# Kernel tuning notes

Hardware: AMD Instinct MI355X
Metric: run time of the kernel (lower is better)

## Reference

```python
import jax, jax.numpy as jnp
import numpy as np

B, P, D, H, BOS, C = 64, 8, 1024, 16, 16, 14
S = BOS + C
L, V, HID = 4, 1024, 2048
DH = D // H
TAU, UW = 1.0, 0.1
SOS_IDX, EOS_IDX = 0, 1


def setup_inputs():
    ks = jax.random.split(jax.random.key(0), 16)
    w = lambda k, s: 0.02 * jax.random.normal(k, s, dtype=jnp.float32)
    return {
        "prototypes": jax.random.normal(ks[0], (B, P, D), jnp.float32),
        "query": jax.random.normal(ks[1], (BOS, D), jnp.float32),
        "ca_wq": w(ks[2], (D, D)), "ca_wk": w(ks[3], (D, D)),
        "ca_wv": w(ks[4], (D, D)), "ca_wo": w(ks[5], (D, D)),
        "ln1_w": jnp.ones((L, D)), "ln1_b": jnp.zeros((L, D)),
        "qkv_w": w(ks[6], (L, D, 3 * D)),
        "attn_out_w": w(ks[7], (L, D, D)),
        "rel_bias": w(ks[8], (L, 2 * S - 1, H)),
        "ln2_w": jnp.ones((L, D)), "ln2_b": jnp.zeros((L, D)),
        "mlp_w1": w(ks[9], (L, D, 2 * HID)),
        "mlp_w2": w(ks[10], (L, HID, D)),
        "lnf_w": jnp.ones((D,)), "lnf_b": jnp.zeros((D,)),
        "vocab_w": w(ks[11], (D, V)), "vocab_b": jnp.zeros((V,)),
        "pos_emb": w(ks[12], (C, D)),
        "tok_emb": w(ks[13], (V, D)),
    }


def _ln(x, w, b):
    m = jnp.mean(x, -1, keepdims=True)
    v = jnp.mean(jnp.square(x - m), -1, keepdims=True)
    return (x - m) * jax.lax.rsqrt(v + 1e-5) * w + b


def _forward(prototypes, query, ca_wq, ca_wk, ca_wv, ca_wo, ln1_w, ln1_b, qkv_w,
             attn_out_w, rel_bias, ln2_w, ln2_b, mlp_w1, mlp_w2, lnf_w, lnf_b,
             vocab_w, vocab_b, pos_emb, tok_emb):
    # cross attention (scaling='d' -> divide by head dim) builds the BOS tokens
    qh = (query @ ca_wq).reshape(BOS, H, DH)                 # shared across batch
    kh = (prototypes @ ca_wk).reshape(B, P, H, DH)
    vh = (prototypes @ ca_wv).reshape(B, P, H, DH)
    att = jax.nn.softmax(jnp.einsum('qhd,bkhd->bhqk', qh, kh) / DH, axis=-1)
    bos = jnp.einsum('bhqk,bkhd->bqhd', att, vh).reshape(B, BOS, D) @ ca_wo

    # learned relative position bias -> (L, H, S, S); causal mask (bidirectional=False)
    ridx = jnp.arange(S)[:, None] - jnp.arange(S)[None, :] + (S - 1)
    bias = jnp.transpose(rel_bias[:, ridx], (0, 3, 1, 2))
    causal = jnp.tril(jnp.ones((S, S), dtype=bool))

    def transformer(x):  # pre-LN encoder, SwiGLU MLP (mlp_ratio=2), eval mode
        for l in range(L):
            h = _ln(x, ln1_w[l], ln1_b[l])
            qkv = (h @ qkv_w[l]).reshape(B, S, 3, H, DH)
            sc = jnp.einsum('bqhd,bkhd->bhqk', qkv[:, :, 0], qkv[:, :, 1]) * (DH ** -0.5) + bias[l]
            a = jax.nn.softmax(jnp.where(causal, sc, -1e30), axis=-1)
            x = x + jnp.einsum('bhqk,bkhd->bqhd', a, qkv[:, :, 2]).reshape(B, S, D) @ attn_out_w[l]
            h = _ln(x, ln2_w[l], ln2_b[l])
            u1, u2 = jnp.split(h @ mlp_w1[l], 2, axis=-1)
            x = x + (jax.nn.silu(u1) * u2) @ mlp_w2[l]
        return _ln(x, lnf_w, lnf_b)

    pos_b = jnp.broadcast_to(pos_emb[None], (B, C, D))
    gkey = jax.random.key(42)

    def step(carry, i):
        spoken, _ = carry
        # slots < i hold embedded spoken tokens, slots >= i hold position embeddings
        mask = (jnp.arange(C) < i)[None, :, None]
        x = jnp.concatenate([bos, jnp.where(mask, spoken, pos_b)], axis=1)
        logits = transformer(x)[:, BOS:, :] @ vocab_w + vocab_b
        g = jax.random.gumbel(jax.random.fold_in(gkey, i), logits.shape, logits.dtype)
        soft = jax.nn.softmax((logits + g) / TAU, axis=-1)
        soft = (1.0 - UW) * soft + UW / V
        hard = jax.nn.one_hot(jnp.argmax(soft, axis=-1), V, dtype=soft.dtype)
        st = hard - jax.lax.stop_gradient(soft) + soft  # straight-through one-hot
        return (st @ tok_emb, st), None

    init = (jnp.zeros((B, C, D), jnp.float32), jnp.zeros((B, C, V), jnp.float32))
    (_, st_last), _ = jax.lax.scan(step, init, jnp.arange(C))
    sos = jnp.zeros((B, 1, V), jnp.float32).at[:, 0, SOS_IDX].set(1.0)
    eos = jnp.zeros((B, 1, V), jnp.float32).at[:, 0, EOS_IDX].set(1.0)
    return jnp.concatenate([sos, st_last, eos], axis=1)


def reference(prototypes, query, ca_wq, ca_wk, ca_wv, ca_wo, ln1_w, ln1_b, qkv_w,
              attn_out_w, rel_bias, ln2_w, ln2_b, mlp_w1, mlp_w2, lnf_w, lnf_b,
              vocab_w, vocab_b, pos_emb, tok_emb):
    return _forward(prototypes, query, ca_wq, ca_wk, ca_wv, ca_wo, ln1_w, ln1_b,
                    qkv_w, attn_out_w, rel_bias, ln2_w, ln2_b, mlp_w1, mlp_w2,
                    lnf_w, lnf_b, vocab_w, vocab_b, pos_emb, tok_emb)
```

## Files before the change

### kernel.cpp

```cpp
#include <hip/hip_runtime.h>
#include <stdint.h>
#include <stddef.h>
#include <math.h>

#define NB   64
#define NP   8
#define ND   1024
#define NH   16
#define NBOS 16
#define NC   14
#define NS   30
#define NL   4
#define NV   1024
#define NHID 2048
#define NDH  64

#define JAX_PARTITIONABLE 1

typedef _Float16 half_t;
typedef _Float16 h4_t __attribute__((ext_vector_type(4)));
typedef _Float16 h8_t __attribute__((ext_vector_type(8)));
typedef float f32x4 __attribute__((ext_vector_type(4)));

__device__ __forceinline__ uint32_t rotl32(uint32_t x, int d) {
  return (x << d) | (x >> (32 - d));
}

__device__ __forceinline__ void threefry2x32(uint32_t k0, uint32_t k1,
                                             uint32_t x0, uint32_t x1,
                                             uint32_t& o0, uint32_t& o1) {
  uint32_t ks2 = k0 ^ k1 ^ 0x1BD11BDAu;
  x0 += k0; x1 += k1;
#define TF_R4(a,b,c,d) \
  x0 += x1; x1 = rotl32(x1,(a)); x1 ^= x0; \
  x0 += x1; x1 = rotl32(x1,(b)); x1 ^= x0; \
  x0 += x1; x1 = rotl32(x1,(c)); x1 ^= x0; \
  x0 += x1; x1 = rotl32(x1,(d)); x1 ^= x0;
  TF_R4(13,15,26,6)  x0 += k1;  x1 += ks2 + 1u;
  TF_R4(17,29,16,24) x0 += ks2; x1 += k0 + 2u;
  TF_R4(13,15,26,6)  x0 += k0;  x1 += k1 + 3u;
  TF_R4(17,29,16,24) x0 += k1;  x1 += ks2 + 4u;
  TF_R4(13,15,26,6)  x0 += ks2; x1 += k0 + 5u;
#undef TF_R4
  o0 = x0; o1 = x1;
}

__global__ __launch_bounds__(256) void k_gemm(
    const float* __restrict__ A, const float* __restrict__ Bm,
    float* __restrict__ Cm, const float* __restrict__ bias,
    int M, int N, int K, int epi) {
  __shared__ __align__(16) float As[16][64];
  __shared__ __align__(16) float Bs[16][64];
  const int tid = threadIdx.x;
  const int tx = tid & 15, ty = tid >> 4;
  const int m0 = blockIdx.y * 64, n0 = blockIdx.x * 64;
  const int lar = tid >> 2, lak = (tid & 3) << 2;
  const int lbk = tid >> 4, lbn = (tid & 15) << 2;
  float acc[4][4] = {};
  for (int kt = 0; kt < K; kt += 16) {
    float4 av = make_float4(0.f, 0.f, 0.f, 0.f);
    if (m0 + lar < M)
      av = *(const float4*)(A + (size_t)(m0 + lar) * K + kt + lak);
    float4 bv4 = make_float4(0.f, 0.f, 0.f, 0.f);
    if (n0 + lbn < N)
      bv4 = *(const float4*)(Bm + (size_t)(kt + lbk) * N + n0 + lbn);
    __syncthreads();
    As[lak + 0][lar] = av.x; As[lak + 1][lar] = av.y;
    As[lak + 2][lar] = av.z; As[lak + 3][lar] = av.w;
    *(float4*)(&Bs[lbk][lbn]) = bv4;
    __syncthreads();
#pragma unroll
    for (int kk = 0; kk < 16; ++kk) {
      float4 a4 = *(const float4*)(&As[kk][ty << 2]);
      float4 b4 = *(const float4*)(&Bs[kk][tx << 2]);
      float ar[4] = {a4.x, a4.y, a4.z, a4.w};
      float br[4] = {b4.x, b4.y, b4.z, b4.w};
#pragma unroll
      for (int i2 = 0; i2 < 4; ++i2)
#pragma unroll
        for (int j2 = 0; j2 < 4; ++j2)
          acc[i2][j2] = fmaf(ar[i2], br[j2], acc[i2][j2]);
    }
  }
#pragma unroll
  for (int i2 = 0; i2 < 4; ++i2) {
    int r = m0 + (ty << 2) + i2;
    if (r >= M) continue;
#pragma unroll
    for (int j2 = 0; j2 < 4; ++j2) {
      int c = n0 + (tx << 2) + j2;
      if (c >= N) continue;
      size_t off = (size_t)r * N + c;
      float val = acc[i2][j2];
      if (epi == 1) val += Cm[off];
      else if (epi == 2) val += bias[c];
      Cm[off] = val;
    }
  }
}

__device__ __forceinline__ void gload16(const void* g, const void* l) {
  __builtin_amdgcn_global_load_lds((const __attribute__((address_space(1))) void*)g,
                                   (__attribute__((address_space(3))) void*)l, 16, 0, 0);
}

__device__ __forceinline__ void xcd_swz(int gx, int gy, int& bx, int& by) {
  const int flat = blockIdx.y * gx + blockIdx.x;
  const int chunk = (gx * gy) >> 3;
  const int myid = (flat & 7) * chunk + (flat >> 3);
  bx = myid / gy;
  by = myid % gy;
}

template<int EPI>
__global__ __launch_bounds__(512) void k_g3(
    const half_t* __restrict__ Ah, const half_t* __restrict__ Al,
    const half_t* __restrict__ Bh, const half_t* __restrict__ Bl,
    float* __restrict__ Cout, half_t* __restrict__ Mh, half_t* __restrict__ Ml,
    int M, int N, int K, int CH) {
  __shared__ __align__(16) half_t sAh[2][4096];
  __shared__ __align__(16) half_t sAl[2][4096];
  __shared__ __align__(16) half_t sBh[2][4096];
  __shared__ __align__(16) half_t sBl[2][4096];
  int bx, by; xcd_swz(gridDim.x, gridDim.y, bx, by);
  const int tid = threadIdx.x;
  const int lane = tid & 63, w = tid >> 6;
  const int wm = w >> 2, wn = w & 3;
  const int m0 = by * 128, n0 = bx * 128;
  const int fr = lane & 15, fq = lane >> 4;
  const int kbeg = blockIdx.z * CH;
  const int kend = (kbeg + CH < K) ? (kbeg + CH) : K;
  f32x4 acc[4][2] = {};
  const int r0 = tid >> 2, ch = (tid & 3) * 8;
  const size_t aB = (size_t)(m0 + r0) * K + ch;
  const size_t bB = (size_t)(n0 + r0) * K + ch;
  const int wb = w * 1024;

  auto STAGE = [&](int buf, int kt) {
    gload16(Ah + aB + kt, (char*)(&sAh[buf][0]) + wb);
    gload16(Al + aB + kt, (char*)(&sAl[buf][0]) + wb);
    gload16(Bh + bB + kt, (char*)(&sBh[buf][0]) + wb);
    gload16(Bl + bB + kt, (char*)(&sBl[buf][0]) + wb);
  };

  STAGE(0, kbeg);
  int cur = 0;
  for (int kt = kbeg; kt < kend; kt += 32) {
    const bool has_next = (kt + 32 < kend);
    if (has_next) {
      STAGE(cur ^ 1, kt + 32);
      asm volatile("s_waitcnt vmcnt(4)" ::: "memory");
    } else {
      asm volatile("s_waitcnt vmcnt(0)" ::: "memory");
    }
    asm volatile("s_barrier" ::: "memory");
    const half_t* bAh = &sAh[cur][0] + (wm * 64 + fr) * 32 + fq * 8;
    const half_t* bAl = &sAl[cur][0] + (wm * 64 + fr) * 32 + fq * 8;
    const half_t* bBh = &sBh[cur][0] + (wn * 32 + fr) * 32 + fq * 8;
    const half_t* bBl = &sBl[cur][0] + (wn * 32 + fr) * 32 + fq * 8;
    h8_t a[4], b[2], t[2];
#pragma unroll
    for (int mi = 0; mi < 4; ++mi) a[mi] = *(const h8_t*)(bAh + mi * 512);
#pragma unroll
    for (int ni = 0; ni < 2; ++ni) b[ni] = *(const h8_t*)(bBh + ni * 512);
#pragma unroll
    for (int mi = 0; mi < 4; ++mi)
#pragma unroll
      for (int ni = 0; ni < 2; ++ni)
        acc[mi][ni] = __builtin_amdgcn_mfma_f32_16x16x32_f16(a[mi], b[ni], acc[mi][ni], 0, 0, 0);
#pragma unroll
    for (int ni = 0; ni < 2; ++ni) t[ni] = *(const h8_t*)(bBl + ni * 512);
#pragma unroll
    for (int mi = 0; mi < 4; ++mi)
#pragma unroll
      for (int ni = 0; ni < 2; ++ni)
        acc[mi][ni] = __builtin_amdgcn_mfma_f32_16x16x32_f16(a[mi], t[ni], acc[mi][ni], 0, 0, 0);
#pragma unroll
    for (int mi = 0; mi < 4; ++mi) a[mi] = *(const h8_t*)(bAl + mi * 512);
    asm volatile("s_barrier" ::: "memory");
#pragma unroll
    for (int mi = 0; mi < 4; ++mi)
#pragma unroll
      for (int ni = 0; ni < 2; ++ni)
        acc[mi][ni] = __builtin_amdgcn_mfma_f32_16x16x32_f16(a[mi], b[ni], acc[mi][ni], 0, 0, 0);
    cur ^= 1;
  }
  const float sc = 1.0f / 1024.0f;
  if (EPI == 0) {
    float* Cz = Cout + (size_t)blockIdx.z * M * N;
#pragma unroll
    for (int mi = 0; mi < 4; ++mi) {
      const int row = m0 + wm * 64 + mi * 16 + fq * 4;
#pragma unroll
      for (int ni = 0; ni < 2; ++ni) {
        const int col = n0 + wn * 32 + ni * 16 + fr;
        float* cp = Cz + (size_t)row * N + col;
#pragma unroll
        for (int j = 0; j < 4; ++j) cp[(size_t)j * N] = acc[mi][ni][j] * sc;
      }
    }
  } else if (EPI == 1) {
    const int hid = ((n0 + wn * 32) >> 1) + fr;
#pragma unroll
    for (int mi = 0; mi < 4; ++mi) {
      const int row = m0 + wm * 64 + mi * 16 + fq * 4;
#pragma unroll
      for (int j = 0; j < 4; ++j) {
        const float u1 = acc[mi][0][j] * sc;
        const float u2 = acc[mi][1][j] * sc;
        const float s = 1.0f / (1.0f + expf(-u1));
        const float y = (u1 * s) * u2 * 16.0f;
        const half_t hv = (half_t)y;
        const size_t off = (size_t)(row + j) * NHID + hid;
        Mh[off] = hv;
        Ml[off] = (half_t)(y - (float)hv);
      }
    }
  } else {
#pragma unroll
    for (int mi = 0; mi < 4; ++mi) {
      const int row = m0 + wm * 64 + mi * 16 + fq * 4;
#pragma unroll
      for (int ni = 0; ni < 2; ++ni) {
        const int col = n0 + wn * 32 + ni * 16 + fr;
#pragma unroll
        for (int j = 0; j < 4; ++j) {
          const float v = acc[mi][ni][j] * sc;
          const half_t hv = (half_t)v;
          const size_t off = (size_t)(row + j) * N + col;
          Mh[off] = hv;
          Ml[off] = (half_t)(v - (float)hv);
        }
      }
    }
  }
}

__global__ __launch_bounds__(256) void k_splitw(
    const float* __restrict__ W, half_t* __restrict__ Th, half_t* __restrict__ Tl,
    int K, int N) {
  __shared__ float t[32][33];
  const int kb = blockIdx.x * 32, nb = blockIdx.y * 32;
  const int tid = threadIdx.x;
  const int rr = tid >> 5, cc = tid & 31;
#pragma unroll
  for (int i = 0; i < 4; ++i)
    t[rr + i * 8][cc] = W[(size_t)(kb + rr + i * 8) * N + nb + cc];
  __syncthreads();
#pragma unroll
  for (int i = 0; i < 4; ++i) {
    const int nr = rr + i * 8;
    const float x = t[cc][nr] * 64.0f;
    const half_t h = (half_t)x;
    const float r = x - (float)h;
    const size_t off = (size_t)(nb + nr) * K + kb + cc;
    Th[off] = h;
    Tl[off] = (half_t)r;
  }
}

__global__ __launch_bounds__(256) void k_splitw_swz(
    const float* __restrict__ W, half_t* __restrict__ Th, half_t* __restrict__ Tl,
    int K, int N) {
  __shared__ float t[32][33];
  const int kb = blockIdx.x * 32, nb = blockIdx.y * 32;
  const int tid = threadIdx.x;
  const int rr = tid >> 5, cc = tid & 31;
#pragma unroll
  for (int i = 0; i < 4; ++i)
    t[rr + i * 8][cc] = W[(size_t)(kb + rr + i * 8) * N + nb + cc];
  __syncthreads();
#pragma unroll
  for (int i = 0; i < 4; ++i) {
    const int n = nb + rr + i * 8;
    const int hid = n & (NHID - 1), half = n >> 11;
    const int p = ((hid >> 4) << 5) + (half << 4) + (hid & 15);
    const float x = t[cc][rr + i * 8] * 64.0f;
    const half_t h = (half_t)x;
    const float r = x - (float)h;
    const size_t off = (size_t)p * K + kb + cc;
    Th[off] = h;
    Tl[off] = (half_t)r;
  }
}

__global__ __launch_bounds__(256) void k_ca_attn(
    const float* __restrict__ qh, const float* __restrict__ kh,
    const float* __restrict__ vh, float* __restrict__ bosw) {
  const int b = blockIdx.x >> 4, h = blockIdx.x & 15;
  __shared__ float q[NBOS][NDH], kk[NP][NDH], vv[NP][NDH], a[NBOS][NP];
  const int tid = threadIdx.x;
  for (int idx = tid; idx < NBOS * NDH; idx += 256) {
    int qi = idx >> 6, d = idx & 63;
    q[qi][d] = qh[(size_t)qi * ND + h * NDH + d];
  }
  for (int idx = tid; idx < NP * NDH; idx += 256) {
    int p = idx >> 6, d = idx & 63;
    kk[p][d] = kh[(size_t)(b * NP + p) * ND + h * NDH + d];
    vv[p][d] = vh[(size_t)(b * NP + p) * ND + h * NDH + d];
  }
  __syncthreads();
  if (tid < NBOS * NP) {
    int qi = tid >> 3, p = tid & 7;
    float dot = 0.f;
    for (int d = 0; d < NDH; ++d) dot = fmaf(q[qi][d], kk[p][d], dot);
    a[qi][p] = dot / 64.0f;
  }
  __syncthreads();
  if (tid < NBOS) {
    float mx = a[tid][0];
    for (int p = 1; p < NP; ++p) mx = fmaxf(mx, a[tid][p]);
    float sum = 0.f;
    for (int p = 0; p < NP; ++p) { float e = expf(a[tid][p] - mx); a[tid][p] = e; sum += e; }
    for (int p = 0; p < NP; ++p) a[tid][p] /= sum;
  }
  __syncthreads();
  for (int idx = tid; idx < NBOS * NDH; idx += 256) {
    int qi = idx >> 6, d = idx & 63;
    float o = 0.f;
    for (int p = 0; p < NP; ++p) o = fmaf(a[qi][p], vv[p][d], o);
    bosw[(size_t)(b * NBOS + qi) * ND + h * NDH + d] = o;
  }
}

__global__ __launch_bounds__(256) void k_attn(
    const float* __restrict__ qkv, const float* __restrict__ relb,
    float* __restrict__ attout) {
  const int b = blockIdx.x >> 4, h = blockIdx.x & 15;
  __shared__ float q[NS][NDH], kk[NS][NDH], vv[NS][NDH];
  __shared__ float a[NS][NS];
  const int tid = threadIdx.x;
  for (int idx = tid; idx < NS * NDH; idx += 256) {
    int s = idx >> 6, d = idx & 63;
    size_t base = ((size_t)(b * NS + s) * 3) * ND + h * NDH + d;
    q[s][d]  = qkv[base];
    kk[s][d] = qkv[base + ND];
    vv[s][d] = qkv[base + 2 * ND];
  }
  __syncthreads();
  for (int idx = tid; idx < NS * NS; idx += 256) {
    int i = idx / NS, j = idx % NS;
    float sc = 0.f;
    if (j <= i) {
      float dot = 0.f;
      for (int d = 0; d < NDH; ++d) dot = fmaf(q[i][d], kk[j][d], dot);
      sc = dot * 0.125f + relb[(size_t)(i - j + NS - 1) * NH + h];
    }
    a[i][j] = sc;
  }
  __syncthreads();
  if (tid < NS) {
    const int i = tid;
    float mx = -INFINITY;
    for (int j = 0; j <= i; ++j) mx = fmaxf(mx, a[i][j]);
    float sum = 0.f;
    for (int j = 0; j <= i; ++j) { float e = expf(a[i][j] - mx); a[i][j] = e; sum += e; }
    for (int j = 0; j <= i; ++j) a[i][j] /= sum;
    for (int j = i + 1; j < NS; ++j) a[i][j] = 0.f;
  }
  __syncthreads();
  for (int idx = tid; idx < NS * NDH; idx += 256) {
    int i = idx >> 6, d = idx & 63;
    float o = 0.f;
    for (int j = 0; j < NS; ++j) o = fmaf(a[i][j], vv[j][d], o);
    attout[(size_t)(b * NS + i) * ND + h * NDH + d] = o;
  }
}

__global__ __launch_bounds__(256) void k_attn16p(
    const half_t* __restrict__ Qh, const half_t* __restrict__ Ql,
    const float* __restrict__ relb,
    half_t* __restrict__ Oh, half_t* __restrict__ Ol, int S) {
  const int b = blockIdx.x >> 4, h = blockIdx.x & 15;
  __shared__ float q[NS][NDH], kk[NS][NDH], vv[NS][NDH];
  __shared__ float a[NS][NS];
  const int tid = threadIdx.x;
  for (int idx = tid; idx < S * NDH; idx += 256) {
    int s = idx >> 6, d = idx & 63;
    size_t base = (size_t)(b * S + s) * 3072 + h * NDH + d;
    q[s][d]  = (float)Qh[base] + (float)Ql[base];
    kk[s][d] = (float)Qh[base + 1024] + (float)Ql[base + 1024];
    vv[s][d] = (float)Qh[base + 2048] + (float)Ql[base + 2048];
  }
  __syncthreads();
  for (int idx = tid; idx < S * S; idx += 256) {
    int i = idx / S, j = idx % S;
    float sc = 0.f;
    if (j <= i) {
      float dot = 0.f;
      for (int d = 0; d < NDH; ++d) dot = fmaf(q[i][d], kk[j][d], dot);
      sc = dot * 0.125f + relb[(size_t)(i - j + NS - 1) * NH + h];
    }
    a[i][j] = sc;
  }
  __syncthreads();
  if (tid < S) {
    const int i = tid;
    float mx = -INFINITY;
    for (int j = 0; j <= i; ++j) mx = fmaxf(mx, a[i][j]);
    float sum = 0.f;
    for (int j = 0; j <= i; ++j) { float e = expf(a[i][j] - mx); a[i][j] = e; sum += e; }
    for (int j = 0; j <= i; ++j) a[i][j] /= sum;
    for (int j = i + 1; j < S; ++j) a[i][j] = 0.f;
  }
  __syncthreads();
  for (int idx = tid; idx < S * NDH; idx += 256) {
    int i = idx >> 6, d = idx & 63;
    float o = 0.f;
    for (int j = 0; j < S; ++j) o = fmaf(a[i][j], vv[j][d], o);
    const float y = o * 16.0f;
    const half_t hv = (half_t)y;
    const size_t off = (size_t)(b * S + i) * ND + h * NDH + d;
    Oh[off] = hv;
    Ol[off] = (half_t)(y - (float)hv);
  }
}

__global__ __launch_bounds__(256) void k_copy_kv(
    const half_t* __restrict__ Qh, const half_t* __restrict__ Ql,
    half_t* __restrict__ Ch, half_t* __restrict__ Cl) {
  const int row = blockIdx.x;
  const int c0 = threadIdx.x * 8;
  const size_t src = (size_t)row * 3072 + 1024 + c0;
  const size_t dst = (size_t)row * 2048 + c0;
  *(h8_t*)(Ch + dst) = *(const h8_t*)(Qh + src);
  *(h8_t*)(Cl + dst) = *(const h8_t*)(Ql + src);
}

__global__ __launch_bounds__(256) void k_attn16c(
    const half_t* __restrict__ Qh, const half_t* __restrict__ Ql,
    const half_t* __restrict__ Ch, const half_t* __restrict__ Cl,
    const float* __restrict__ relb,
    half_t* __restrict__ Oh, half_t* __restrict__ Ol, int ncur) {
  const int b = blockIdx.x >> 4, h = blockIdx.x & 15;
  const int S = NBOS + ncur;
  __shared__ float q[NC][NDH], kk[NS][NDH], vv[NS][NDH];
  __shared__ float a[NC][NS];
  const int tid = threadIdx.x;
  for (int idx = tid; idx < ncur * NDH; idx += 256) {
    int c = idx >> 6, d = idx & 63;
    size_t base = (size_t)(b * ncur + c) * 3072 + h * NDH + d;
    q[c][d] = (float)Qh[base] + (float)Ql[base];
  }
  for (int idx = tid; idx < S * NDH; idx += 256) {
    int j = idx >> 6, d = idx & 63;
    if (j < NBOS) {
      size_t r = (size_t)(b * NBOS + j) * 2048 + h * NDH + d;
      kk[j][d] = (float)Ch[r] + (float)Cl[r];
      vv[j][d] = (float)Ch[r + 1024] + (float)Cl[r + 1024];
    } else {
      size_t base = (size_t)(b * ncur + (j - NBOS)) * 3072 + h * NDH + d;
      kk[j][d] = (float)Qh[base + 1024] + (float)Ql[base + 1024];
      vv[j][d] = (float)Qh[base + 2048] + (float)Ql[base + 2048];
    }
  }
  __syncthreads();
  for (int idx = tid; idx < ncur * S; idx += 256) {
    int c = idx / S, j = idx % S;
    const int s = NBOS + c;
    float sc = 0.f;
    if (j <= s) {
      float dot = 0.f;
      for (int d = 0; d < NDH; ++d) dot = fmaf(q[c][d], kk[j][d], dot);
      sc = dot * 0.125f + relb[(size_t)(s - j + NS - 1) * NH + h];
    }
    a[c][j] = sc;
  }
  __syncthreads();
  if (tid < ncur) {
    const int c = tid, s = NBOS + c;
    float mx = -INFINITY;
    for (int j = 0; j <= s; ++j) mx = fmaxf(mx, a[c][j]);
    float sum = 0.f;
    for (int j = 0; j <= s; ++j) { float e = expf(a[c][j] - mx); a[c][j] = e; sum += e; }
    for (int j = 0; j <= s; ++j) a[c][j] /= sum;
    for (int j = s + 1; j < S; ++j) a[c][j] = 0.f;
  }
  __syncthreads();
  for (int idx = tid; idx < ncur * NDH; idx += 256) {
    int c = idx >> 6, d = idx & 63;
    float o = 0.f;
    for (int j = 0; j < S; ++j) o = fmaf(a[c][j], vv[j][d], o);
    const float y = o * 16.0f;
    const half_t hv = (half_t)y;
    const size_t off = (size_t)(b * ncur + c) * ND + h * NDH + d;
    Oh[off] = hv;
    Ol[off] = (half_t)(y - (float)hv);
  }
}

__device__ __forceinline__ float block_sum(float val, float* sbuf) {
  for (int off = 32; off > 0; off >>= 1) val += __shfl_down(val, off, 64);
  const int wid = threadIdx.x >> 6;
  if ((threadIdx.x & 63) == 0) sbuf[wid] = val;
  __syncthreads();
  if (threadIdx.x == 0) sbuf[0] = sbuf[0] + sbuf[1] + sbuf[2] + sbuf[3];
  __syncthreads();
  float r = sbuf[0];
  __syncthreads();
  return r;
}

__device__ __forceinline__ void ln_core_emit16(
    float4 x4, const float* w, const float* bvec, float* sbuf,
    half_t* Oh, half_t* Ol, size_t rowoff, int d0) {
  float mean = block_sum(x4.x + x4.y + x4.z + x4.w, sbuf) * (1.0f / 1024.0f);
  float dx0 = x4.x - mean, dx1 = x4.y - mean, dx2 = x4.z - mean, dx3 = x4.w - mean;
  float var = block_sum(dx0*dx0 + dx1*dx1 + dx2*dx2 + dx3*dx3, sbuf) * (1.0f / 1024.0f);
  float rs = 1.0f / sqrtf(var + 1e-5f);
  float4 w4 = *(const float4*)(w + d0);
  float4 b4 = *(const float4*)(bvec + d0);
  float y0 = (dx0 * rs * w4.x + b4.x) * 16.0f;
  float y1 = (dx1 * rs * w4.y + b4.y) * 16.0f;
  float y2 = (dx2 * rs * w4.z + b4.z) * 16.0f;
  float y3 = (dx3 * rs * w4.w + b4.w) * 16.0f;
  h4_t vh, vl;
  vh.x = (half_t)y0; vl.x = (half_t)(y0 - (float)vh.x);
  vh.y = (half_t)y1; vl.y = (half_t)(y1 - (float)vh.y);
  vh.z = (half_t)y2; vl.z = (half_t)(y2 - (float)vh.z);
  vh.w = (half_t)y3; vl.w = (half_t)(y3 - (float)vh.w);
  *(h4_t*)(Oh + rowoff + d0) = vh;
  *(h4_t*)(Ol + rowoff + d0) = vl;
}

__global__ __launch_bounds__(256) void k_ln(
    const float* __restrict__ in, const float* __restrict__ w,
    const float* __restrict__ bvec, float* __restrict__ out) {
  __shared__ float sbuf[4];
  const size_t row = blockIdx.x;
  const int d0 = threadIdx.x << 2;
  float4 x4 = *(const float4*)(in + row * ND + d0);
  float mean = block_sum(x4.x + x4.y + x4.z + x4.w, sbuf) * (1.0f / 1024.0f);
  float dx0 = x4.x - mean, dx1 = x4.y - mean, dx2 = x4.z - mean, dx3 = x4.w - mean;
  float var = block_sum(dx0*dx0 + dx1*dx1 + dx2*dx2 + dx3*dx3, sbuf) * (1.0f / 1024.0f);
  float rs = 1.0f / sqrtf(var + 1e-5f);
  float4 w4 = *(const float4*)(w + d0);
  float4 b4 = *(const float4*)(bvec + d0);
  float4 o;
  o.x = dx0 * rs * w4.x + b4.x;
  o.y = dx1 * rs * w4.y + b4.y;
  o.z = dx2 * rs * w4.z + b4.z;
  o.w = dx3 * rs * w4.w + b4.w;
  *(float4*)(out + row * ND + d0) = o;
}

template<int WRITEX>
__global__ __launch_bounds__(256) void k_red_ln(
    const float* __restrict__ parts, float* __restrict__ X,
    const float* __restrict__ w, const float* __restrict__ bvec,
    half_t* __restrict__ Oh, half_t* __restrict__ Ol, int Mp) {
  __shared__ float sbuf[4];
  const size_t row = blockIdx.x;
  const int d0 = threadIdx.x << 2;
  const size_t off = row * ND + d0;
  const size_t MN = (size_t)Mp * 1024;
  float4 x4 = *(const float4*)(X + off);
  float4 p0 = *(const float4*)(parts + off);
  float4 p1 = *(const float4*)(parts + MN + off);
  float4 p2 = *(const float4*)(parts + 2 * MN + off);
  x4.x += p0.x + p1.x + p2.x; x4.y += p0.y + p1.y + p2.y;
  x4.z += p0.z + p1.z + p2.z; x4.w += p0.w + p1.w + p2.w;
  if (WRITEX) *(float4*)(X + off) = x4;
  ln_core_emit16(x4, w, bvec, sbuf, Oh, Ol, row * ND, d0);
}

__global__ __launch_bounds__(256) void k_lnf(
    const float* __restrict__ x, const float* __restrict__ w,
    const float* __restrict__ bvec, float* __restrict__ out) {
  __shared__ float sbuf[4];
  const int blk = blockIdx.x;
  const int b = blk / NC, c = blk % NC;
  const size_t row = (size_t)b * NS + NBOS + c;
  const int d0 = threadIdx.x << 2;
  float4 x4 = *(const float4*)(x + row * ND + d0);
  float mean = block_sum(x4.x + x4.y + x4.z + x4.w, sbuf) * (1.0f / 1024.0f);
  float dx0 = x4.x - mean, dx1 = x4.y - mean, dx2 = x4.z - mean, dx3 = x4.w - mean;
  float var = block_sum(dx0*dx0 + dx1*dx1 + dx2*dx2 + dx3*dx3, sbuf) * (1.0f / 1024.0f);
  float rs = 1.0f / sqrtf(var + 1e-5f);
  float4 w4 = *(const float4*)(w + d0);
  float4 b4 = *(const float4*)(bvec + d0);
  float4 o;
  o.x = dx0 * rs * w4.x + b4.x;
  o.y = dx1 * rs * w4.y + b4.y;
  o.z = dx2 * rs * w4.z + b4.z;
  o.w = dx3 * rs * w4.w + b4.w;
  *(float4*)(out + (size_t)blk * ND + d0) = o;
}

__device__ __forceinline__ float4 build_row(
    const float* bos, const float* pos_emb, const float* tok_emb,
    const int* tok, const float* stval, int b, int s, int d0, int step) {
  float4 o;
  if (s < NBOS) {
    o = *(const float4*)(bos + (size_t)(b * NBOS + s) * ND + d0);
  } else {
    int j = s - NBOS;
    if (j < step) {
      float sv = stval[b * NC + j];
      int t = tok[b * NC + j];
      float4 e = *(const float4*)(tok_emb + (size_t)t * ND + d0);
      o.x = sv * e.x; o.y = sv * e.y; o.z = sv * e.z; o.w = sv * e.w;
    } else {
      o = *(const float4*)(pos_emb + (size_t)j * ND + d0);
    }
  }
  return o;
}

__global__ __launch_bounds__(256) void k_build_x(
    const float* __restrict__ bos, const float* __restrict__ pos_emb,
    const float* __restrict__ tok_emb, const int* __restrict__ tok,
    const float* __restrict__ stval, float* __restrict__ x, int step) {
  const int row = blockIdx.x;
  const int b = row / NS, s = row % NS;
  const int d0 = threadIdx.x << 2;
  float4 o = build_row(bos, pos_emb, tok_emb, tok, stval, b, s, d0, step);
  *(float4*)(x + (size_t)row * ND + d0) = o;
}

__global__ __launch_bounds__(256) void k_build_ln(
    const float* __restrict__ bos, const float* __restrict__ pos_emb,
    const float* __restrict__ tok_emb, const int* __restrict__ tok,
    const float* __restrict__ stval, const float* __restrict__ w,
    const float* __restrict__ bvec, float* __restrict__ x,
    half_t* __restrict__ Oh, half_t* __restrict__ Ol, int step, int S) {
  __shared__ float sbuf[4];
  const int row = blockIdx.x;
  const int b = row / S, s = row % S;
  const int d0 = threadIdx.x << 2;
  float4 o = build_row(bos, pos_emb, tok_emb, tok, stval, b, s, d0, step);
  *(float4*)(x + (size_t)row * ND + d0) = o;
  ln_core_emit16(o, w, bvec, sbuf, Oh, Ol, (size_t)row * ND, d0);
}

__global__ __launch_bounds__(256) void k_build_ln_c(
    const float* __restrict__ pos_emb, const float* __restrict__ tok_emb,
    const int* __restrict__ tok, const float* __restrict__ stval,
    const float* __restrict__ w, const float* __restrict__ bvec,
    float* __restrict__ x, half_t* __restrict__ Oh, half_t* __restrict__ Ol,
    int step, int ncur) {
  __shared__ float sbuf[4];
  const int row = blockIdx.x;
  const int b = row / ncur, c = row % ncur;
  const int d0 = threadIdx.x << 2;
  float4 o;
  if (c < step) {
    float sv = stval[b * NC + c];
    int t = tok[b * NC + c];
    float4 e = *(const float4*)(tok_emb + (size_t)t * ND + d0);
    o.x = sv * e.x; o.y = sv * e.y; o.z = sv * e.z; o.w = sv * e.w;
  } else {
    o = *(const float4*)(pos_emb + (size_t)c * ND + d0);
  }
  *(float4*)(x + (size_t)row * ND + d0) = o;
  ln_core_emit16(o, w, bvec, sbuf, Oh, Ol, (size_t)row * ND, d0);
}

__global__ __launch_bounds__(256) void k_swiglu(const float* __restrict__ u,
                                                float* __restrict__ m) {
  const size_t idx4 = (size_t)blockIdx.x * 256 + threadIdx.x;
  const size_t row = idx4 >> 9;
  const size_t c0 = (idx4 & 511) << 2;
  const float* ur = u + row * (2 * NHID);
  float4 a4 = *(const float4*)(ur + c0);
  float4 b4 = *(const float4*)(ur + NHID + c0);
  float4 o;
  { float s = 1.0f / (1.0f + expf(-a4.x)); o.x = (a4.x * s) * b4.x; }
  { float s = 1.0f / (1.0f + expf(-a4.y)); o.y = (a4.y * s) * b4.y; }
  { float s = 1.0f / (1.0f + expf(-a4.z)); o.z = (a4.z * s) * b4.z; }
  { float s = 1.0f / (1.0f + expf(-a4.w)); o.w = (a4.w * s) * b4.w; }
  *(float4*)(m + row * NHID + c0) = o;
}

template<int GRED>
__global__ __launch_bounds__(256) void k_gumbel_t(
    const float* __restrict__ logits, const float* __restrict__ vb,
    int* __restrict__ tok, float* __restrict__ stval, float* __restrict__ out,
    int step, int finalstep, int ncur, int Mp) {
  const int blk = blockIdx.x;
  const int b = blk / ncur, c = blk % ncur;
  const int tid = threadIdx.x;
  uint32_t fk0, fk1;
  threefry2x32(0u, 42u, 0u, (uint32_t)step, fk0, fk1);
  const float* zrow = logits + (size_t)blk * NV;
  const size_t MN = (size_t)Mp * 1024;
  float y[4];
  float bv = -INFINITY; int bi = 0;
#pragma unroll
  for (int j = 0; j < 4; ++j) {
    const int v = tid + (j << 8);
    const uint32_t idx = (uint32_t)(b * NC + c) * 1024u + (uint32_t)v;
    uint32_t o0, o1, bits;
#if JAX_PARTITIONABLE
    threefry2x32(fk0, fk1, 0u, idx, o0, o1);
    bits = o0 ^ o1;
#else
    const uint32_t half = (uint32_t)(NB * NC * NV / 2);
    uint32_t jj = (idx < half) ? idx : idx - half;
    threefry2x32(fk0, fk1, jj, jj + half, o0, o1);
    bits = (idx < half) ? o0 : o1;
#endif
    float f = __uint_as_float(0x3F800000u | (bits >> 9)) - 1.0f;
    float uu = (f == 0.0f) ? 1.17549435e-38f : f;
    float g = -logf(-logf(uu));
    float z;
    if (GRED) z = zrow[v] + zrow[MN + v] + zrow[2 * MN + v] + vb[v];
    else      z = zrow[v];
    float yv = z + g;
    y[j] = yv;
    if (yv > bv) { bv = yv; bi = v; }
  }
  __shared__ float swv[4]; __shared__ int swi[4];
  __shared__ float s_ymax; __shared__ int s_arg;
  for (int off = 32; off > 0; off >>= 1) {
    float ov = __shfl_down(bv, off, 64);
    int   oi = __shfl_down(bi, off, 64);
    if (ov > bv || (ov == bv && oi < bi)) { bv = ov; bi = oi; }
  }
  if ((tid & 63) == 0) { swv[tid >> 6] = bv; swi[tid >> 6] = bi; }
  __syncthreads();
  if (tid == 0) {
    float mv = swv[0]; int mi = swi[0];
    for (int w2 = 1; w2 < 4; ++w2)
      if (swv[w2] > mv || (swv[w2] == mv && swi[w2] < mi)) { mv = swv[w2]; mi = swi[w2]; }
    s_ymax = mv; s_arg = mi;
  }
  __syncthreads();
  const float ymax = s_ymax;
  float es = 0.f;
#pragma unroll
  for (int j = 0; j < 4; ++j) es += expf(y[j] - ymax);
  __shared__ float sbuf2[4]; __shared__ float s_es;
  for (int off = 32; off > 0; off >>= 1) es += __shfl_down(es, off, 64);
  if ((tid & 63) == 0) sbuf2[tid >> 6] = es;
  __syncthreads();
  if (tid == 0) s_es = sbuf2[0] + sbuf2[1] + sbuf2[2] + sbuf2[3];
  __syncthreads();
  const float esum = s_es;
  const float sprob = 0.9f * (1.0f / esum) + (0.1f / 1024.0f);
  const float stv = (1.0f - sprob) + sprob;
  if (tid == 0) { tok[b * NC + c] = s_arg; stval[b * NC + c] = stv; }
  if (finalstep) {
    float* orow = out + ((size_t)b * (NC + 2) + 1 + c) * NV;
#pragma unroll
    for (int j = 0; j < 4; ++j) {
      const int v = tid + (j << 8);
      orow[v] = (v == s_arg) ? stv : 0.0f;
    }
  }
}

__global__ __launch_bounds__(256) void k_out_init(float* __restrict__ out) {
  const int b = blockIdx.x;
  const int tid = threadIdx.x;
#pragma unroll
  for (int j = 0; j < 4; ++j) {
    const int v = tid + (j << 8);
    out[((size_t)b * (NC + 2) + 0) * NV + v]      = (v == 0) ? 1.0f : 0.0f;
    out[((size_t)b * (NC + 2) + NC + 1) * NV + v] = (v == 1) ? 1.0f : 0.0f;
  }
}

extern "C" void kernel_launch(void* const* d_in, const int* in_sizes, int n_in,
                              void* d_out, int out_size, void* d_ws, size_t ws_size,
                              hipStream_t stream) {
  (void)in_sizes; (void)n_in; (void)out_size;
  const float* prototypes = (const float*)d_in[0];
  const float* query      = (const float*)d_in[1];
  const float* ca_wq      = (const float*)d_in[2];
  const float* ca_wk      = (const float*)d_in[3];
  const float* ca_wv      = (const float*)d_in[4];
  const float* ca_wo      = (const float*)d_in[5];
  const float* ln1_w      = (const float*)d_in[6];
  const float* ln1_b      = (const float*)d_in[7];
  const float* qkv_w      = (const float*)d_in[8];
  const float* attn_out_w = (const float*)d_in[9];
  const float* rel_bias   = (const float*)d_in[10];
  const float* ln2_w      = (const float*)d_in[11];
  const float* ln2_b      = (const float*)d_in[12];
  const float* mlp_w1     = (const float*)d_in[13];
  const float* mlp_w2     = (const float*)d_in[14];
  const float* lnf_w      = (const float*)d_in[15];
  const float* lnf_b      = (const float*)d_in[16];
  const float* vocab_w    = (const float*)d_in[17];
  const float* vocab_b    = (const float*)d_in[18];
  const float* pos_emb    = (const float*)d_in[19];
  const float* tok_emb    = (const float*)d_in[20];
  float* out = (float*)d_out;

  dim3 thr(256);
  dim3 thr512(512);
  const size_t NEED = 234889216ull;

  if (ws_size >= NEED) {
    char* p = (char*)d_ws;
    auto alloc = [&](size_t bytes) { char* r = p; p += (bytes + 255) & ~(size_t)255; return r; };
    half_t *WqH[NL], *WqL[NL], *WaH[NL], *WaL[NL], *W1H[NL], *W1L[NL], *W2H[NL], *W2L[NL];
    for (int l = 0; l < NL; ++l) {
      WqH[l] = (half_t*)alloc(3072 * 1024 * 2);
      WqL[l] = (half_t*)alloc(3072 * 1024 * 2);
      WaH[l] = (half_t*)alloc(1024 * 1024 * 2);
      WaL[l] = (half_t*)alloc(1024 * 1024 * 2);
      W1H[l] = (half_t*)alloc(4096 * 1024 * 2);
      W1L[l] = (half_t*)alloc(4096 * 1024 * 2);
      W2H[l] = (half_t*)alloc(1024 * 2048 * 2);
      W2L[l] = (half_t*)alloc(1024 * 2048 * 2);
    }
    half_t* WvH = (half_t*)alloc(1024 * 1024 * 2);
    half_t* WvL = (half_t*)alloc(1024 * 1024 * 2);
    half_t *KVh[NL], *KVl[NL];
    for (int l = 0; l < NL; ++l) {
      KVh[l] = (half_t*)alloc(1024 * 2048 * 2);
      KVl[l] = (half_t*)alloc(1024 * 2048 * 2);
    }
    half_t* Hh  = (half_t*)alloc(1024 * 1024 * 2);
    half_t* Hl  = (half_t*)alloc(1024 * 1024 * 2);
    float*  X   = (float*)alloc(1024 * 1024 * 4);
    char*  QKVr = alloc(12582912);
    half_t* Mh  = (half_t*)alloc(1024 * 2048 * 2);
    half_t* Ml  = (half_t*)alloc(1024 * 2048 * 2);
    float* STV  = (float*)alloc(4096);
    int*   TOK  = (int*)alloc(4096);
    float* PARTS = (float*)QKVr;
    half_t* QKVh = (half_t*)QKVr;
    half_t* QKVl = QKVh + (size_t)1024 * 3072;
    float* BOSb  = (float*)Mh;

    for (int l = 0; l < NL; ++l) {
      k_splitw<<<dim3(32, 96), thr, 0, stream>>>(qkv_w + (size_t)l * ND * 3 * ND, WqH[l], WqL[l], 1024, 3072);
      k_splitw<<<dim3(32, 32), thr, 0, stream>>>(attn_out_w + (size_t)l * ND * ND, WaH[l], WaL[l], 1024, 1024);
      k_splitw_swz<<<dim3(32, 128), thr, 0, stream>>>(mlp_w1 + (size_t)l * ND * 2 * NHID, W1H[l], W1L[l], 1024, 4096);
      k_splitw<<<dim3(64, 32), thr, 0, stream>>>(mlp_w2 + (size_t)l * NHID * ND, W2H[l], W2L[l], 2048, 1024);
    }
    k_splitw<<<dim3(32, 32), thr, 0, stream>>>(vocab_w, WvH, WvL, 1024, 1024);

    float* QH = (float*)QKVr;
    float* KH = (float*)QKVr + 16384;
    float* VH = (float*)QKVr + 540672;
    float* BOSW = (float*)QKVr + 1064960;
    k_gemm<<<dim3(16, 1),  thr, 0, stream>>>(query,      ca_wq, QH,   nullptr, NBOS,    ND, ND, 0);
    k_gemm<<<dim3(16, 8),  thr, 0, stream>>>(prototypes, ca_wk, KH,   nullptr, NB * NP, ND, ND, 0);
    k_gemm<<<dim3(16, 8),  thr, 0, stream>>>(prototypes, ca_wv, VH,   nullptr, NB * NP, ND, ND, 0);
    k_ca_attn<<<dim3(NB * NH), thr, 0, stream>>>(QH, KH, VH, BOSW);
    k_gemm<<<dim3(16, 16), thr, 0, stream>>>(BOSW, ca_wo, BOSb, nullptr, NB * NBOS, ND, ND, 0);
    k_out_init<<<dim3(NB), thr, 0, stream>>>(out);

    k_build_ln<<<dim3(1024), thr, 0, stream>>>(BOSb, pos_emb, tok_emb, TOK, STV,
                                               ln1_w, ln1_b, X, Hh, Hl, 0, NBOS);
    for (int l = 0; l < NL; ++l) {
      k_g3<2><<<dim3(24, 8, 1), thr512, 0, stream>>>(Hh, Hl, WqH[l], WqL[l], nullptr, QKVh, QKVl,
                                                     1024, 3072, 1024, 1024);
      k_copy_kv<<<dim3(1024), thr, 0, stream>>>(QKVh, QKVl, KVh[l], KVl[l]);
      k_attn16p<<<dim3(NB * NH), thr, 0, stream>>>(QKVh, QKVl, rel_bias + (size_t)l * (2 * NS - 1) * NH,
                                                   Hh, Hl, NBOS);
      k_g3<0><<<dim3(8, 8, 3), thr512, 0, stream>>>(Hh, Hl, WaH[l], WaL[l], PARTS, nullptr, nullptr,
                                                    1024, 1024, 1024, 352);
      k_red_ln<1><<<dim3(1024), thr, 0, stream>>>(PARTS, X, ln2_w + l * ND, ln2_b + l * ND, Hh, Hl, 1024);
      k_g3<1><<<dim3(32, 8, 1), thr512, 0, stream>>>(Hh, Hl, W1H[l], W1L[l], nullptr, Mh, Ml,
                                                     1024, 4096, 1024, 1024);
      k_g3<0><<<dim3(8, 8, 3), thr512, 0, stream>>>(Mh, Ml, W2H[l], W2L[l], PARTS, nullptr, nullptr,
                                                    1024, 1024, 2048, 704);
      if (l < NL - 1)
        k_red_ln<1><<<dim3(1024), thr, 0, stream>>>(PARTS, X, ln1_w + (l + 1) * ND, ln1_b + (l + 1) * ND,
                                                    Hh, Hl, 1024);
    }

    for (int i = 0; i < NC; ++i) {
      const int ncur = i + 1;
      const int Mv = NB * ncur;
      const int MP = (Mv + 127) & ~127;
      const int gy = MP / 128;

      k_build_ln_c<<<dim3(Mv), thr, 0, stream>>>(pos_emb, tok_emb, TOK, STV,
                                                 ln1_w, ln1_b, X, Hh, Hl, i, ncur);
      for (int l = 0; l < NL; ++l) {
        k_g3<2><<<dim3(24, gy, 1), thr512, 0, stream>>>(Hh, Hl, WqH[l], WqL[l], nullptr, QKVh, QKVl,
                                                        MP, 3072, 1024, 1024);
        k_attn16c<<<dim3(NB * NH), thr, 0, stream>>>(QKVh, QKVl, KVh[l], KVl[l],
                                                     rel_bias + (size_t)l * (2 * NS - 1) * NH,
                                                     Hh, Hl, ncur);
        k_g3<0><<<dim3(8, gy, 3), thr512, 0, stream>>>(Hh, Hl, WaH[l], WaL[l], PARTS, nullptr, nullptr,
                                                       MP, 1024, 1024, 352);
        k_red_ln<1><<<dim3(Mv), thr, 0, stream>>>(PARTS, X, ln2_w + l * ND, ln2_b + l * ND, Hh, Hl, MP);
        k_g3<1><<<dim3(32, gy, 1), thr512, 0, stream>>>(Hh, Hl, W1H[l], W1L[l], nullptr, Mh, Ml,
                                                        MP, 4096, 1024, 1024);
        k_g3<0><<<dim3(8, gy, 3), thr512, 0, stream>>>(Mh, Ml, W2H[l], W2L[l], PARTS, nullptr, nullptr,
                                                       MP, 1024, 2048, 704);
        if (l < NL - 1)
          k_red_ln<1><<<dim3(Mv), thr, 0, stream>>>(PARTS, X, ln1_w + (l + 1) * ND, ln1_b + (l + 1) * ND,
                                                    Hh, Hl, MP);
        else
          k_red_ln<0><<<dim3(Mv), thr, 0, stream>>>(PARTS, X, lnf_w, lnf_b, Hh, Hl, MP);
      }
      k_g3<0><<<dim3(8, gy, 3), thr512, 0, stream>>>(Hh, Hl, WvH, WvL, PARTS, nullptr, nullptr,
                                                     MP, 1024, 1024, 352);
      k_gumbel_t<1><<<dim3(Mv), thr, 0, stream>>>(PARTS, vocab_b, TOK, STV, out, i,
                                                  (i == NC - 1) ? 1 : 0, ncur, MP);
    }
    return;
  }

  float* ws = (float*)d_ws;
  float* BOSW = ws + 0;
  float* BOSb = ws + 1048576;
  float* QH   = ws + 2097152;
  float* KH   = ws + 2113536;
  float* VH   = ws + 2637824;
  float* X    = ws + 3162112;
  float* Hb   = ws + 5128192;
  float* HL   = Hb;
  float* LG   = Hb + 917504;
  float* QKV  = ws + 7094272;
  float* U    = QKV;
  float* ATT  = ws + 14958592;
  float* Mb   = ATT;
  float* STV  = ws + 18890752;
  int*   TOK  = (int*)(ws + 18891648);

  k_gemm<<<dim3(16, 1),  thr, 0, stream>>>(query,      ca_wq, QH,   nullptr, NBOS,    ND, ND, 0);
  k_gemm<<<dim3(16, 8),  thr, 0, stream>>>(prototypes, ca_wk, KH,   nullptr, NB * NP, ND, ND, 0);
  k_gemm<<<dim3(16, 8),  thr, 0, stream>>>(prototypes, ca_wv, VH,   nullptr, NB * NP, ND, ND, 0);
  k_ca_attn<<<dim3(NB * NH), thr, 0, stream>>>(QH, KH, VH, BOSW);
  k_gemm<<<dim3(16, 16), thr, 0, stream>>>(BOSW, ca_wo, BOSb, nullptr, NB * NBOS, ND, ND, 0);
  k_out_init<<<dim3(NB), thr, 0, stream>>>(out);

  for (int i = 0; i < NC; ++i) {
    k_build_x<<<dim3(NB * NS), thr, 0, stream>>>(BOSb, pos_emb, tok_emb, TOK, STV, X, i);
    for (int l = 0; l < NL; ++l) {
      k_ln<<<dim3(NB * NS), thr, 0, stream>>>(X, ln1_w + l * ND, ln1_b + l * ND, Hb);
      k_gemm<<<dim3(48, 30), thr, 0, stream>>>(Hb, qkv_w + (size_t)l * ND * 3 * ND, QKV,
                                               nullptr, NB * NS, 3 * ND, ND, 0);
      k_attn<<<dim3(NB * NH), thr, 0, stream>>>(QKV, rel_bias + (size_t)l * (2 * NS - 1) * NH, ATT);
      k_gemm<<<dim3(16, 30), thr, 0, stream>>>(ATT, attn_out_w + (size_t)l * ND * ND, X,
                                               nullptr, NB * NS, ND, ND, 1);
      k_ln<<<dim3(NB * NS), thr, 0, stream>>>(X, ln2_w + l * ND, ln2_b + l * ND, Hb);
      k_gemm<<<dim3(64, 30), thr, 0, stream>>>(Hb, mlp_w1 + (size_t)l * ND * 2 * NHID, U,
                                               nullptr, NB * NS, 2 * NHID, ND, 0);
      k_swiglu<<<dim3(3840), thr, 0, stream>>>(U, Mb);
      k_gemm<<<dim3(16, 30), thr, 0, stream>>>(Mb, mlp_w2 + (size_t)l * NHID * ND, X,
                                               nullptr, NB * NS, ND, NHID, 1);
    }
    k_lnf<<<dim3(NB * NC), thr, 0, stream>>>(X, lnf_w, lnf_b, HL);
    k_gemm<<<dim3(16, 14), thr, 0, stream>>>(HL, vocab_w, LG, vocab_b, NB * NC, NV, ND, 2);
    k_gumbel_t<0><<<dim3(NB * NC), thr, 0, stream>>>(LG, nullptr, TOK, STV, out, i,
                                                     (i == NC - 1) ? 1 : 0, NC, 896);
  }
}
```

Measured before the change: 8.853 ms.

## Fuse decode-loop kernels into one cooperative persistent megakernel with grid syncs

The 14-step autoregressive decode loop, previously about a hundred small kernel launches per step, becomes a single cooperative kernel of 256 blocks. Each block loops over GEMM tiles, attention items and LN rows, with grid-wide syncs between phases. The GEMM tile is reworked for 256 threads, with each wave computing a 64x64 subtile and dynamic shared memory passed in. This removes launch overhead and idle gaps between the tiny decode-step kernels. The cost is grid-sync latency, a fixed grid size that may underfill some GEMM phases, and lower occupancy from 64KB of LDS per block.

```diff
diff --git a/kernel.cpp b/kernel.cpp
--- a/kernel.cpp
+++ b/kernel.cpp
@@ -1,7 +1,10 @@
 #include <hip/hip_runtime.h>
+#include <hip/hip_cooperative_groups.h>
 #include <stdint.h>
 #include <stddef.h>
 #include <math.h>
+
+namespace cg = cooperative_groups;
 
 #define NB   64
 #define NP   8
@@ -113,107 +116,121 @@
 }
 
 template<int EPI>
-__global__ __launch_bounds__(512) void k_g3(
+__device__ void dev_g3(char* sm, int bx, int by, int bz,
     const half_t* __restrict__ Ah, const half_t* __restrict__ Al,
     const half_t* __restrict__ Bh, const half_t* __restrict__ Bl,
     float* __restrict__ Cout, half_t* __restrict__ Mh, half_t* __restrict__ Ml,
     int M, int N, int K, int CH) {
-  __shared__ __align__(16) half_t sAh[2][4096];
-  __shared__ __align__(16) half_t sAl[2][4096];
-  __shared__ __align__(16) half_t sBh[2][4096];
-  __shared__ __align__(16) half_t sBl[2][4096];
-  int bx, by; xcd_swz(gridDim.x, gridDim.y, bx, by);
+  half_t* sAh = (half_t*)sm;
+  half_t* sAl = (half_t*)(sm + 16384);
+  half_t* sBh = (half_t*)(sm + 32768);
+  half_t* sBl = (half_t*)(sm + 49152);
   const int tid = threadIdx.x;
   const int lane = tid & 63, w = tid >> 6;
-  const int wm = w >> 2, wn = w & 3;
+  const int wm = w >> 1, wn = w & 1;
   const int m0 = by * 128, n0 = bx * 128;
   const int fr = lane & 15, fq = lane >> 4;
-  const int kbeg = blockIdx.z * CH;
+  const int kbeg = bz * CH;
   const int kend = (kbeg + CH < K) ? (kbeg + CH) : K;
-  f32x4 acc[4][2] = {};
+  f32x4 acc[4][4] = {};
   const int r0 = tid >> 2, ch = (tid & 3) * 8;
-  const size_t aB = (size_t)(m0 + r0) * K + ch;
-  const size_t bB = (size_t)(n0 + r0) * K + ch;
+  const size_t aB0 = (size_t)(m0 + r0) * K + ch;
+  const size_t aB1 = (size_t)(m0 + 64 + r0) * K + ch;
+  const size_t bB0 = (size_t)(n0 + r0) * K + ch;
+  const size_t bB1 = (size_t)(n0 + 64 + r0) * K + ch;
   const int wb = w * 1024;
 
   auto STAGE = [&](int buf, int kt) {
-    gload16(Ah + aB + kt, (char*)(&sAh[buf][0]) + wb);
-    gload16(Al + aB + kt, (char*)(&sAl[buf][0]) + wb);
-    gload16(Bh + bB + kt, (char*)(&sBh[buf][0]) + wb);
-    gload16(Bl + bB + kt, (char*)(&sBl[buf][0]) + wb);
+    char* dAh = (char*)sAh + buf * 8192 + wb;
+    char* dAl = (char*)sAl + buf * 8192 + wb;
+    char* dBh = (char*)sBh + buf * 8192 + wb;
+    char* dBl = (char*)sBl + buf * 8192 + wb;
+    gload16(Ah + aB0 + kt, dAh);
+    gload16(Ah + aB1 + kt, dAh + 4096);
+    gload16(Al + aB0 + kt, dAl);
+    gload16(Al + aB1 + kt, dAl + 4096);
+    gload16(Bh + bB0 + kt, dBh);
+    gload16(Bh + bB1 + kt, dBh + 4096);
+    gload16(Bl + bB0 + kt, dBl);
+    gload16(Bl + bB1 + kt, dBl + 4096);
   };
 
+  __syncthreads();
   STAGE(0, kbeg);
   int cur = 0;
   for (int kt = kbeg; kt < kend; kt += 32) {
     const bool has_next = (kt + 32 < kend);
     if (has_next) {
       STAGE(cur ^ 1, kt + 32);
-      asm volatile("s_waitcnt vmcnt(4)" ::: "memory");
+      asm volatile("s_waitcnt vmcnt(8)" ::: "memory");
     } else {
       asm volatile("s_waitcnt vmcnt(0)" ::: "memory");
     }
     asm volatile("s_barrier" ::: "memory");
-    const half_t* bAh = &sAh[cur][0] + (wm * 64 + fr) * 32 + fq * 8;
-    const half_t* bAl = &sAl[cur][0] + (wm * 64 + fr) * 32 + fq * 8;
-    const half_t* bBh = &sBh[cur][0] + (wn * 32 + fr) * 32 + fq * 8;
-    const half_t* bBl = &sBl[cur][0] + (wn * 32 + fr) * 32 + fq * 8;
-    h8_t a[4], b[2], t[2];
-#pragma unroll
-    for (int mi = 0; mi < 4; ++mi) a[mi] = *(const h8_t*)(bAh + mi * 512);
-#pragma unroll
-    for (int ni = 0; ni < 2; ++ni) b[ni] = *(const h8_t*)(bBh + ni * 512);
+    const half_t* pAh = sAh + cur * 4096 + (wm * 64 + fr) * 32 + fq * 8;
+    const half_t* pAl = sAl + cur * 4096 + (wm * 64 + fr) * 32 + fq * 8;
+    const half_t* pBh = sBh + cur * 4096 + (wn * 64 + fr) * 32 + fq * 8;
+    const half_t* pBl = sBl + cur * 4096 + (wn * 64 + fr) * 32 + fq * 8;
+    h8_t a[4], b[4], t[4];
+#pragma unroll
+    for (int i = 0; i < 4; ++i) a[i] = *(const h8_t*)(pAh + i * 512);
+#pragma unroll
+    for (int i = 0; i < 4; ++i) b[i] = *(const h8_t*)(pBh + i * 512);
 #pragma unroll
     for (int mi = 0; mi < 4; ++mi)
 #pragma unroll
-      for (int ni = 0; ni < 2; ++ni)
+      for (int ni = 0; ni < 4; ++ni)
         acc[mi][ni] = __builtin_amdgcn_mfma_f32_16x16x32_f16(a[mi], b[ni], acc[mi][ni], 0, 0, 0);
 #pragma unroll
-    for (int ni = 0; ni < 2; ++ni) t[ni] = *(const h8_t*)(bBl + ni * 512);
+    for (int i = 0; i < 4; ++i) t[i] = *(const h8_t*)(pBl + i * 512);
 #pragma unroll
     for (int mi = 0; mi < 4; ++mi)
 #pragma unroll
-      for (int ni = 0; ni < 2; ++ni)
+      for (int ni = 0; ni < 4; ++ni)
         acc[mi][ni] = __builtin_amdgcn_mfma_f32_16x16x32_f16(a[mi], t[ni], acc[mi][ni], 0, 0, 0);
 #pragma unroll
-    for (int mi = 0; mi < 4; ++mi) a[mi] = *(const h8_t*)(bAl + mi * 512);
+    for (int i = 0; i < 4; ++i) a[i] = *(const h8_t*)(pAl + i * 512);
     asm volatile("s_barrier" ::: "memory");
 #pragma unroll
     for (int mi = 0; mi < 4; ++mi)
 #pragma unroll
-      for (int ni = 0; ni < 2; ++ni)
+      for (int ni = 0; ni < 4; ++ni)
         acc[mi][ni] = __builtin_amdgcn_mfma_f32_16x16x32_f16(a[mi], b[ni], acc[mi][ni], 0, 0, 0);
     cur ^= 1;
   }
   const float sc = 1.0f / 1024.0f;
   if (EPI == 0) {
-    float* Cz = Cout + (size_t)blockIdx.z * M * N;
+    float* Cz = Cout + (size_t)bz * M * N;
 #pragma unroll
     for (int mi = 0; mi < 4; ++mi) {
       const int row = m0 + wm * 64 + mi * 16 + fq * 4;
 #pragma unroll
-      for (int ni = 0; ni < 2; ++ni) {
-        const int col = n0 + wn * 32 + ni * 16 + fr;
+      for (int ni = 0; ni < 4; ++ni) {
+        const int col = n0 + wn * 64 + ni * 16 + fr;
         float* cp = Cz + (size_t)row * N + col;
 #pragma unroll
         for (int j = 0; j < 4; ++j) cp[(size_t)j * N] = acc[mi][ni][j] * sc;
       }
     }
   } else if (EPI == 1) {
-    const int hid = ((n0 + wn * 32) >> 1) + fr;
+    const int h0 = (n0 >> 1) + wn * 32;
 #pragma unroll
     for (int mi = 0; mi < 4; ++mi) {
       const int row = m0 + wm * 64 + mi * 16 + fq * 4;
 #pragma unroll
-      for (int j = 0; j < 4; ++j) {
-        const float u1 = acc[mi][0][j] * sc;
-        const float u2 = acc[mi][1][j] * sc;
-        const float s = 1.0f / (1.0f + expf(-u1));
-        const float y = (u1 * s) * u2 * 16.0f;
-        const half_t hv = (half_t)y;
-        const size_t off = (size_t)(row + j) * NHID + hid;
-        Mh[off] = hv;
-        Ml[off] = (half_t)(y - (float)hv);
+      for (int p = 0; p < 2; ++p) {
+        const int hcol = h0 + p * 16 + fr;
+#pragma unroll
+        for (int j = 0; j < 4; ++j) {
+          const float u1 = acc[mi][2 * p][j] * sc;
+          const float u2 = acc[mi][2 * p + 1][j] * sc;
+          const float s = 1.0f / (1.0f + expf(-u1));
+          const float y = (u1 * s) * u2 * 16.0f;
+          const half_t hv = (half_t)y;
+          const size_t off = (size_t)(row + j) * NHID + hcol;
+          Mh[off] = hv;
+          Ml[off] = (half_t)(y - (float)hv);
+        }
       }
     }
   } else {
@@ -221,8 +238,8 @@
     for (int mi = 0; mi < 4; ++mi) {
       const int row = m0 + wm * 64 + mi * 16 + fq * 4;
 #pragma unroll
-      for (int ni = 0; ni < 2; ++ni) {
-        const int col = n0 + wn * 32 + ni * 16 + fr;
+      for (int ni = 0; ni < 4; ++ni) {
+        const int col = n0 + wn * 64 + ni * 16 + fr;
 #pragma unroll
         for (int j = 0; j < 4; ++j) {
           const float v = acc[mi][ni][j] * sc;
@@ -234,6 +251,17 @@
       }
     }
   }
+}
+
+template<int EPI>
+__global__ __launch_bounds__(256) void k_g3(
+    const half_t* __restrict__ Ah, const half_t* __restrict__ Al,
+    const half_t* __restrict__ Bh, const half_t* __restrict__ Bl,
+    float* __restrict__ Cout, half_t* __restrict__ Mh, half_t* __restrict__ Ml,
+    int M, int N, int K, int CH) {
+  __shared__ __align__(16) char sm[65536];
+  int bx, by; xcd_swz(gridDim.x, gridDim.y, bx, by);
+  dev_g3<EPI>(sm, bx, by, blockIdx.z, Ah, Al, Bh, Bl, Cout, Mh, Ml, M, N, K, CH);
 }
 
 __global__ __launch_bounds__(256) void k_splitw(
@@ -425,68 +453,6 @@
   const size_t dst = (size_t)row * 2048 + c0;
   *(h8_t*)(Ch + dst) = *(const h8_t*)(Qh + src);
   *(h8_t*)(Cl + dst) = *(const h8_t*)(Ql + src);
-}
-
-__global__ __launch_bounds__(256) void k_attn16c(
-    const half_t* __restrict__ Qh, const half_t* __restrict__ Ql,
-    const half_t* __restrict__ Ch, const half_t* __restrict__ Cl,
-    const float* __restrict__ relb,
-    half_t* __restrict__ Oh, half_t* __restrict__ Ol, int ncur) {
-  const int b = blockIdx.x >> 4, h = blockIdx.x & 15;
-  const int S = NBOS + ncur;
-  __shared__ float q[NC][NDH], kk[NS][NDH], vv[NS][NDH];
-  __shared__ float a[NC][NS];
-  const int tid = threadIdx.x;
-  for (int idx = tid; idx < ncur * NDH; idx += 256) {
-    int c = idx >> 6, d = idx & 63;
-    size_t base = (size_t)(b * ncur + c) * 3072 + h * NDH + d;
-    q[c][d] = (float)Qh[base] + (float)Ql[base];
-  }
-  for (int idx = tid; idx < S * NDH; idx += 256) {
-    int j = idx >> 6, d = idx & 63;
-    if (j < NBOS) {
-      size_t r = (size_t)(b * NBOS + j) * 2048 + h * NDH + d;
-      kk[j][d] = (float)Ch[r] + (float)Cl[r];
-      vv[j][d] = (float)Ch[r + 1024] + (float)Cl[r + 1024];
-    } else {
-      size_t base = (size_t)(b * ncur + (j - NBOS)) * 3072 + h * NDH + d;
-      kk[j][d] = (float)Qh[base + 1024] + (float)Ql[base + 1024];
-      vv[j][d] = (float)Qh[base + 2048] + (float)Ql[base + 2048];
-    }
-  }
-  __syncthreads();
-  for (int idx = tid; idx < ncur * S; idx += 256) {
-    int c = idx / S, j = idx % S;
-    const int s = NBOS + c;
-    float sc = 0.f;
-    if (j <= s) {
-      float dot = 0.f;
-      for (int d = 0; d < NDH; ++d) dot = fmaf(q[c][d], kk[j][d], dot);
-      sc = dot * 0.125f + relb[(size_t)(s - j + NS - 1) * NH + h];
-    }
-    a[c][j] = sc;
-  }
-  __syncthreads();
-  if (tid < ncur) {
-    const int c = tid, s = NBOS + c;
-    float mx = -INFINITY;
-    for (int j = 0; j <= s; ++j) mx = fmaxf(mx, a[c][j]);
-    float sum = 0.f;
-    for (int j = 0; j <= s; ++j) { float e = expf(a[c][j] - mx); a[c][j] = e; sum += e; }
-    for (int j = 0; j <= s; ++j) a[c][j] /= sum;
-    for (int j = s + 1; j < S; ++j) a[c][j] = 0.f;
-  }
-  __syncthreads();
-  for (int idx = tid; idx < ncur * NDH; idx += 256) {
-    int c = idx >> 6, d = idx & 63;
-    float o = 0.f;
-    for (int j = 0; j < S; ++j) o = fmaf(a[c][j], vv[j][d], o);
-    const float y = o * 16.0f;
-    const half_t hv = (half_t)y;
-    const size_t off = (size_t)(b * ncur + c) * ND + h * NDH + d;
-    Oh[off] = hv;
-    Ol[off] = (half_t)(y - (float)hv);
-  }
 }
 
 __device__ __forceinline__ float block_sum(float val, float* sbuf) {
@@ -523,6 +489,206 @@
   *(h4_t*)(Ol + rowoff + d0) = vl;
 }
 
+__device__ void dev_build_ln_c(char* sm, int row,
+    const float* pos_emb, const float* tok_emb, const int* tok,
+    const float* stval, const float* w, const float* bvec,
+    float* x, half_t* Oh, half_t* Ol, int step, int ncur) {
+  float* sbuf = (float*)sm;
+  const int b = row / ncur, c = row % ncur;
+  const int d0 = threadIdx.x << 2;
+  float4 o;
+  if (c < step) {
+    float sv = stval[b * NC + c];
+    int t = tok[b * NC + c];
+    float4 e = *(const float4*)(tok_emb + (size_t)t * ND + d0);
+    o.x = sv * e.x; o.y = sv * e.y; o.z = sv * e.z; o.w = sv * e.w;
+  } else {
+    o = *(const float4*)(pos_emb + (size_t)c * ND + d0);
+  }
+  *(float4*)(x + (size_t)row * ND + d0) = o;
+  ln_core_emit16(o, w, bvec, sbuf, Oh, Ol, (size_t)row * ND, d0);
+}
+
+__device__ void dev_attn16c(char* sm, int item,
+    const half_t* Qh, const half_t* Ql,
+    const half_t* Ch, const half_t* Cl,
+    const float* relb, half_t* Oh, half_t* Ol, int ncur) {
+  const int b = item >> 4, h = item & 15;
+  const int S = NBOS + ncur;
+  float* q  = (float*)sm;
+  float* kk = q + NC * NDH;
+  float* vv = kk + NS * NDH;
+  float* a  = vv + NS * NDH;
+  const int tid = threadIdx.x;
+  __syncthreads();
+  for (int idx = tid; idx < ncur * NDH; idx += 256) {
+    int c = idx >> 6, d = idx & 63;
+    size_t base = (size_t)(b * ncur + c) * 3072 + h * NDH + d;
+    q[c * NDH + d] = (float)Qh[base] + (float)Ql[base];
+  }
+  for (int idx = tid; idx < S * NDH; idx += 256) {
+    int j = idx >> 6, d = idx & 63;
+    if (j < NBOS) {
+      size_t r = (size_t)(b * NBOS + j) * 2048 + h * NDH + d;
+      kk[j * NDH + d] = (float)Ch[r] + (float)Cl[r];
+      vv[j * NDH + d] = (float)Ch[r + 1024] + (float)Cl[r + 1024];
+    } else {
+      size_t base = (size_t)(b * ncur + (j - NBOS)) * 3072 + h * NDH + d;
+      kk[j * NDH + d] = (float)Qh[base + 1024] + (float)Ql[base + 1024];
+      vv[j * NDH + d] = (float)Qh[base + 2048] + (float)Ql[base + 2048];
+    }
+  }
+  __syncthreads();
+  for (int idx = tid; idx < ncur * S; idx += 256) {
+    int c = idx / S, j = idx % S;
+    const int s = NBOS + c;
+    float sc = 0.f;
+    if (j <= s) {
+      float dot = 0.f;
+      for (int d = 0; d < NDH; ++d) dot = fmaf(q[c * NDH + d], kk[j * NDH + d], dot);
+      sc = dot * 0.125f + relb[(size_t)(s - j + NS - 1) * NH + h];
+    }
+    a[c * NS + j] = sc;
+  }
+  __syncthreads();
+  if (tid < ncur) {
+    const int c = tid, s = NBOS + c;
+    float mx = -INFINITY;
+    for (int j = 0; j <= s; ++j) mx = fmaxf(mx, a[c * NS + j]);
+    float sum = 0.f;
+    for (int j = 0; j <= s; ++j) { float e = expf(a[c * NS + j] - mx); a[c * NS + j] = e; sum += e; }
+    for (int j = 0; j <= s; ++j) a[c * NS + j] /= sum;
+    for (int j = s + 1; j < S; ++j) a[c * NS + j] = 0.f;
+  }
+  __syncthreads();
+  for (int idx = tid; idx < ncur * NDH; idx += 256) {
+    int c = idx >> 6, d = idx & 63;
+    float o = 0.f;
+    for (int j = 0; j < S; ++j) o = fmaf(a[c * NS + j], vv[j * NDH + d], o);
+    const float y = o * 16.0f;
+    const half_t hv = (half_t)y;
+    const size_t off = (size_t)(b * ncur + c) * ND + h * NDH + d;
+    Oh[off] = hv;
+    Ol[off] = (half_t)(y - (float)hv);
+  }
+}
+
+template<int WRITEX>
+__device__ void dev_red_ln(char* sm, int rowi,
+    const float* parts, float* X, const float* w, const float* bvec,
+    half_t* Oh, half_t* Ol, int Mp) {
+  float* sbuf = (float*)sm;
+  const size_t row = rowi;
+  const int d0 = threadIdx.x << 2;
+  const size_t off = row * ND + d0;
+  const size_t MN = (size_t)Mp * 1024;
+  float4 x4 = *(const float4*)(X + off);
+  float4 p0 = *(const float4*)(parts + off);
+  float4 p1 = *(const float4*)(parts + MN + off);
+  float4 p2 = *(const float4*)(parts + 2 * MN + off);
+  x4.x += p0.x + p1.x + p2.x; x4.y += p0.y + p1.y + p2.y;
+  x4.z += p0.z + p1.z + p2.z; x4.w += p0.w + p1.w + p2.w;
+  if (WRITEX) *(float4*)(X + off) = x4;
+  ln_core_emit16(x4, w, bvec, sbuf, Oh, Ol, row * ND, d0);
+}
+
+__device__ void dev_gumbel(char* sm, int blk,
+    const float* logits, const float* vb, int* tok, float* stval,
+    float* out, int step, int finalstep, int ncur, int Mp) {
+  float* swv  = (float*)sm;
+  int*   swi  = (int*)(sm + 16);
+  float* sbuf2 = (float*)(sm + 32);
+  float* sder = (float*)(sm + 48);
+  const int b = blk / ncur, c = blk % ncur;
+  const int tid = threadIdx.x;
+  __syncthreads();
+  uint32_t fk0, fk1;
+  threefry2x32(0u, 42u, 0u, (uint32_t)step, fk0, fk1);
+  const float* zrow = logits + (size_t)blk * NV;
+  const size_t MN = (size_t)Mp * 1024;
+  float y[4];
+  float bv = -INFINITY; int bi = 0;
+#pragma unroll
+  for (int j = 0; j < 4; ++j) {
+    const int v = tid + (j << 8);
+    const uint32_t idx = (uint32_t)(b * NC + c) * 1024u + (uint32_t)v;
+    uint32_t o0, o1, bits;
+#if JAX_PARTITIONABLE
+    threefry2x32(fk0, fk1, 0u, idx, o0, o1);
+    bits = o0 ^ o1;
+#else
+    const uint32_t half = (uint32_t)(NB * NC * NV / 2);
+    uint32_t jj = (idx < half) ? idx : idx - half;
+    threefry2x32(fk0, fk1, jj, jj + half, o0, o1);
+    bits = (idx < half) ? o0 : o1;
+#endif
+    float f = __uint_as_float(0x3F800000u | (bits >> 9)) - 1.0f;
+    float uu = (f == 0.0f) ? 1.17549435e-38f : f;
+    float g = -logf(-logf(uu));
+    float z = zrow[v] + zrow[MN + v] + zrow[2 * MN + v] + vb[v];
+    float yv = z + g;
+    y[j] = yv;
+    if (yv > bv) { bv = yv; bi = v; }
+  }
+  for (int off = 32; off > 0; off >>= 1) {
+    float ov = __shfl_down(bv, off, 64);
+    int   oi = __shfl_down(bi, off, 64);
+    if (ov > bv || (ov == bv && oi < bi)) { bv = ov; bi = oi; }
+  }
+  if ((tid & 63) == 0) { swv[tid >> 6] = bv; swi[tid >> 6] = bi; }
+  __syncthreads();
+  if (tid == 0) {
+    float mv = swv[0]; int mi = swi[0];
+    for (int w2 = 1; w2 < 4; ++w2)
+      if (swv[w2] > mv || (swv[w2] == mv && swi[w2] < mi)) { mv = swv[w2]; mi = swi[w2]; }
+    sder[0] = mv; ((int*)sder)[1] = mi;
+  }
+  __syncthreads();
+  const float ymax = sder[0];
+  const int s_arg = ((int*)sder)[1];
+  float es = 0.f;
+#pragma unroll
+  for (int j = 0; j < 4; ++j) es += expf(y[j] - ymax);
+  for (int off = 32; off > 0; off >>= 1) es += __shfl_down(es, off, 64);
+  if ((tid & 63) == 0) sbuf2[tid >> 6] = es;
+  __syncthreads();
+  if (tid == 0) sder[2] = sbuf2[0] + sbuf2[1] + sbuf2[2] + sbuf2[3];
+  __syncthreads();
+  const float esum = sder[2];
+  const float sprob = 0.9f * (1.0f / esum) + (0.1f / 1024.0f);
+  const float stv = (1.0f - sprob) + sprob;
+  if (tid == 0) { tok[b * NC + c] = s_arg; stval[b * NC + c] = stv; }
+  if (finalstep) {
+    float* orow = out + ((size_t)b * (NC + 2) + 1 + c) * NV;
+#pragma unroll
+    for (int j = 0; j < 4; ++j) {
+      const int v = tid + (j << 8);
+      orow[v] = (v == s_arg) ? stv : 0.0f;
+    }
+  }
+}
+
+__global__ __launch_bounds__(256) void k_build_ln(
+    const float* __restrict__ bos, const float* __restrict__ w,
+    const float* __restrict__ bvec, float* __restrict__ x,
+    half_t* __restrict__ Oh, half_t* __restrict__ Ol) {
+  __shared__ float sbuf[4];
+  const int row = blockIdx.x;
+  const int d0 = threadIdx.x << 2;
+  float4 o = *(const float4*)(bos + (size_t)row * ND + d0);
+  *(float4*)(x + (size_t)row * ND + d0) = o;
+  ln_core_emit16(o, w, bvec, sbuf, Oh, Ol, (size_t)row * ND, d0);
+}
+
+template<int WRITEX>
+__global__ __launch_bounds__(256) void k_red_ln(
+    const float* __restrict__ parts, float* __restrict__ X,
+    const float* __restrict__ w, const float* __restrict__ bvec,
+    half_t* __restrict__ Oh, half_t* __restrict__ Ol, int Mp) {
+  __shared__ float sbuf[4];
+  dev_red_ln<WRITEX>((char*)sbuf, blockIdx.x, parts, X, w, bvec, Oh, Ol, Mp);
+}
+
 __global__ __launch_bounds__(256) void k_ln(
     const float* __restrict__ in, const float* __restrict__ w,
     const float* __restrict__ bvec, float* __restrict__ out) {
@@ -542,26 +708,6 @@
   o.z = dx2 * rs * w4.z + b4.z;
   o.w = dx3 * rs * w4.w + b4.w;
   *(float4*)(out + row * ND + d0) = o;
-}
-
-template<int WRITEX>
-__global__ __launch_bounds__(256) void k_red_ln(
-    const float* __restrict__ parts, float* __restrict__ X,
-    const float* __restrict__ w, const float* __restrict__ bvec,
-    half_t* __restrict__ Oh, half_t* __restrict__ Ol, int Mp) {
-  __shared__ float sbuf[4];
-  const size_t row = blockIdx.x;
-  const int d0 = threadIdx.x << 2;
-  const size_t off = row * ND + d0;
-  const size_t MN = (size_t)Mp * 1024;
-  float4 x4 = *(const float4*)(X + off);
-  float4 p0 = *(const float4*)(parts + off);
-  float4 p1 = *(const float4*)(parts + MN + off);
-  float4 p2 = *(const float4*)(parts + 2 * MN + off);
-  x4.x += p0.x + p1.x + p2.x; x4.y += p0.y + p1.y + p2.y;
-  x4.z += p0.z + p1.z + p2.z; x4.w += p0.w + p1.w + p2.w;
-  if (WRITEX) *(float4*)(X + off) = x4;
-  ln_core_emit16(x4, w, bvec, sbuf, Oh, Ol, row * ND, d0);
 }
 
 __global__ __launch_bounds__(256) void k_lnf(
@@ -618,44 +764,6 @@
   *(float4*)(x + (size_t)row * ND + d0) = o;
 }
 
-__global__ __launch_bounds__(256) void k_build_ln(
-    const float* __restrict__ bos, const float* __restrict__ pos_emb,
-    const float* __restrict__ tok_emb, const int* __restrict__ tok,
-    const float* __restrict__ stval, const float* __restrict__ w,
-    const float* __restrict__ bvec, float* __restrict__ x,
-    half_t* __restrict__ Oh, half_t* __restrict__ Ol, int step, int S) {
-  __shared__ float sbuf[4];
-  const int row = blockIdx.x;
-  const int b = row / S, s = row % S;
-  const int d0 = threadIdx.x << 2;
-  float4 o = build_row(bos, pos_emb, tok_emb, tok, stval, b, s, d0, step);
-  *(float4*)(x + (size_t)row * ND + d0) = o;
-  ln_core_emit16(o, w, bvec, sbuf, Oh, Ol, (size_t)row * ND, d0);
-}
-
-__global__ __launch_bounds__(256) void k_build_ln_c(
-    const float* __restrict__ pos_emb, const float* __restrict__ tok_emb,
-    const int* __restrict__ tok, const float* __restrict__ stval,
-    const float* __restrict__ w, const float* __restrict__ bvec,
-    float* __restrict__ x, half_t* __restrict__ Oh, half_t* __restrict__ Ol,
-    int step, int ncur) {
-  __shared__ float sbuf[4];
-  const int row = blockIdx.x;
-  const int b = row / ncur, c = row % ncur;
-  const int d0 = threadIdx.x << 2;
-  float4 o;
-  if (c < step) {
-    float sv = stval[b * NC + c];
-    int t = tok[b * NC + c];
-    float4 e = *(const float4*)(tok_emb + (size_t)t * ND + d0);
-    o.x = sv * e.x; o.y = sv * e.y; o.z = sv * e.z; o.w = sv * e.w;
-  } else {
-    o = *(const float4*)(pos_emb + (size_t)c * ND + d0);
-  }
-  *(float4*)(x + (size_t)row * ND + d0) = o;
-  ln_core_emit16(o, w, bvec, sbuf, Oh, Ol, (size_t)row * ND, d0);
-}
-
 __global__ __launch_bounds__(256) void k_swiglu(const float* __restrict__ u,
                                                 float* __restrict__ m) {
   const size_t idx4 = (size_t)blockIdx.x * 256 + threadIdx.x;
@@ -672,24 +780,21 @@
   *(float4*)(m + row * NHID + c0) = o;
 }
 
-template<int GRED>
-__global__ __launch_bounds__(256) void k_gumbel_t(
-    const float* __restrict__ logits, const float* __restrict__ vb,
-    int* __restrict__ tok, float* __restrict__ stval, float* __restrict__ out,
-    int step, int finalstep, int ncur, int Mp) {
+__global__ __launch_bounds__(256) void k_gumbel_f(
+    const float* __restrict__ logits, int* __restrict__ tok,
+    float* __restrict__ stval, float* __restrict__ out,
+    int step, int finalstep) {
   const int blk = blockIdx.x;
-  const int b = blk / ncur, c = blk % ncur;
   const int tid = threadIdx.x;
   uint32_t fk0, fk1;
   threefry2x32(0u, 42u, 0u, (uint32_t)step, fk0, fk1);
   const float* zrow = logits + (size_t)blk * NV;
-  const size_t MN = (size_t)Mp * 1024;
   float y[4];
   float bv = -INFINITY; int bi = 0;
 #pragma unroll
   for (int j = 0; j < 4; ++j) {
     const int v = tid + (j << 8);
-    const uint32_t idx = (uint32_t)(b * NC + c) * 1024u + (uint32_t)v;
+    const uint32_t idx = (uint32_t)blk * 1024u + (uint32_t)v;
     uint32_t o0, o1, bits;
 #if JAX_PARTITIONABLE
     threefry2x32(fk0, fk1, 0u, idx, o0, o1);
@@ -703,10 +808,7 @@
     float f = __uint_as_float(0x3F800000u | (bits >> 9)) - 1.0f;
     float uu = (f == 0.0f) ? 1.17549435e-38f : f;
     float g = -logf(-logf(uu));
-    float z;
-    if (GRED) z = zrow[v] + zrow[MN + v] + zrow[2 * MN + v] + vb[v];
-    else      z = zrow[v];
-    float yv = z + g;
+    float yv = zrow[v] + g;
     y[j] = yv;
     if (yv > bv) { bv = yv; bi = v; }
   }
@@ -739,8 +841,9 @@
   const float esum = s_es;
   const float sprob = 0.9f * (1.0f / esum) + (0.1f / 1024.0f);
   const float stv = (1.0f - sprob) + sprob;
-  if (tid == 0) { tok[b * NC + c] = s_arg; stval[b * NC + c] = stv; }
+  if (tid == 0) { tok[blk] = s_arg; stval[blk] = stv; }
   if (finalstep) {
+    const int b = blk / NC, c = blk % NC;
     float* orow = out + ((size_t)b * (NC + 2) + 1 + c) * NV;
 #pragma unroll
     for (int j = 0; j < 4; ++j) {
@@ -758,6 +861,103 @@
     const int v = tid + (j << 8);
     out[((size_t)b * (NC + 2) + 0) * NV + v]      = (v == 0) ? 1.0f : 0.0f;
     out[((size_t)b * (NC + 2) + NC + 1) * NV + v] = (v == 1) ? 1.0f : 0.0f;
+  }
+}
+
+struct MegaP {
+  const half_t *WqH0, *WqH1, *WqH2, *WqH3;
+  const half_t *WqL0, *WqL1, *WqL2, *WqL3;
+  const half_t *WaH0, *WaH1, *WaH2, *WaH3;
+  const half_t *WaL0, *WaL1, *WaL2, *WaL3;
+  const half_t *W1H0, *W1H1, *W1H2, *W1H3;
+  const half_t *W1L0, *W1L1, *W1L2, *W1L3;
+  const half_t *W2H0, *W2H1, *W2H2, *W2H3;
+  const half_t *W2L0, *W2L1, *W2L2, *W2L3;
+  const half_t *WvH, *WvL;
+  const half_t *KVh0, *KVh1, *KVh2, *KVh3;
+  const half_t *KVl0, *KVl1, *KVl2, *KVl3;
+  half_t *Hh, *Hl;
+  float* X;
+  half_t *QKVh, *QKVl;
+  float* PARTS;
+  half_t *Mh, *Ml;
+  const float *ln1_w, *ln1_b, *ln2_w, *ln2_b, *lnf_w, *lnf_b;
+  const float *vocab_b, *rel_bias, *pos_emb, *tok_emb;
+  float* STV; int* TOK; float* out;
+};
+
+__global__ __launch_bounds__(256) void k_mega(MegaP P) {
+  cg::grid_group gg = cg::this_grid();
+  __shared__ __align__(16) char sm[65536];
+  const int bid = blockIdx.x, nbk = gridDim.x;
+  const half_t* WqH[NL] = {P.WqH0, P.WqH1, P.WqH2, P.WqH3};
+  const half_t* WqL[NL] = {P.WqL0, P.WqL1, P.WqL2, P.WqL3};
+  const half_t* WaH[NL] = {P.WaH0, P.WaH1, P.WaH2, P.WaH3};
+  const half_t* WaL[NL] = {P.WaL0, P.WaL1, P.WaL2, P.WaL3};
+  const half_t* W1H[NL] = {P.W1H0, P.W1H1, P.W1H2, P.W1H3};
+  const half_t* W1L[NL] = {P.W1L0, P.W1L1, P.W1L2, P.W1L3};
+  const half_t* W2H[NL] = {P.W2H0, P.W2H1, P.W2H2, P.W2H3};
+  const half_t* W2L[NL] = {P.W2L0, P.W2L1, P.W2L2, P.W2L3};
+  const half_t* KVh[NL] = {P.KVh0, P.KVh1, P.KVh2, P.KVh3};
+  const half_t* KVl[NL] = {P.KVl0, P.KVl1, P.KVl2, P.KVl3};
+
+  for (int i = 0; i < NC; ++i) {
+    const int ncur = i + 1;
+    const int Mv = NB * ncur;
+    const int MP = (Mv + 127) & ~127;
+    const int gy = MP >> 7;
+    for (int r = bid; r < Mv; r += nbk)
+      dev_build_ln_c(sm, r, P.pos_emb, P.tok_emb, P.TOK, P.STV,
+                     P.ln1_w, P.ln1_b, P.X, P.Hh, P.Hl, i, ncur);
+    __threadfence(); gg.sync();
+    for (int l = 0; l < NL; ++l) {
+      int nt = 24 * gy;
+      for (int t = bid; t < nt; t += nbk)
+        dev_g3<2>(sm, t % 24, t / 24, 0, P.Hh, P.Hl, WqH[l], WqL[l],
+                  nullptr, P.QKVh, P.QKVl, MP, 3072, 1024, 1024);
+      __threadfence(); gg.sync();
+      for (int t = bid; t < NB * NH; t += nbk)
+        dev_attn16c(sm, t, P.QKVh, P.QKVl, KVh[l], KVl[l],
+                    P.rel_bias + (size_t)l * (2 * NS - 1) * NH, P.Hh, P.Hl, ncur);
+      __threadfence(); gg.sync();
+      nt = 8 * gy * 3;
+      for (int t = bid; t < nt; t += nbk)
+        dev_g3<0>(sm, t % 8, (t / 8) % gy, t / (8 * gy), P.Hh, P.Hl, WaH[l], WaL[l],
+                  P.PARTS, nullptr, nullptr, MP, 1024, 1024, 352);
+      __threadfence(); gg.sync();
+      for (int r = bid; r < Mv; r += nbk)
+        dev_red_ln<1>(sm, r, P.PARTS, P.X, P.ln2_w + l * ND, P.ln2_b + l * ND,
+                      P.Hh, P.Hl, MP);
+      __threadfence(); gg.sync();
+      nt = 32 * gy;
+      for (int t = bid; t < nt; t += nbk)
+        dev_g3<1>(sm, t % 32, t / 32, 0, P.Hh, P.Hl, W1H[l], W1L[l],
+                  nullptr, P.Mh, P.Ml, MP, 4096, 1024, 1024);
+      __threadfence(); gg.sync();
+      nt = 8 * gy * 3;
+      for (int t = bid; t < nt; t += nbk)
+        dev_g3<0>(sm, t % 8, (t / 8) % gy, t / (8 * gy), P.Mh, P.Ml, W2H[l], W2L[l],
+                  P.PARTS, nullptr, nullptr, MP, 1024, 2048, 704);
+      __threadfence(); gg.sync();
+      if (l < NL - 1) {
+        for (int r = bid; r < Mv; r += nbk)
+          dev_red_ln<1>(sm, r, P.PARTS, P.X, P.ln1_w + (l + 1) * ND,
+                        P.ln1_b + (l + 1) * ND, P.Hh, P.Hl, MP);
+      } else {
+        for (int r = bid; r < Mv; r += nbk)
+          dev_red_ln<0>(sm, r, P.PARTS, P.X, P.lnf_w, P.lnf_b, P.Hh, P.Hl, MP);
+      }
+      __threadfence(); gg.sync();
+    }
+    int nt = 8 * gy * 3;
+    for (int t = bid; t < nt; t += nbk)
+      dev_g3<0>(sm, t % 8, (t / 8) % gy, t / (8 * gy), P.Hh, P.Hl, P.WvH, P.WvL,
+                P.PARTS, nullptr, nullptr, MP, 1024, 1024, 352);
+    __threadfence(); gg.sync();
+    for (int t = bid; t < Mv; t += nbk)
+      dev_gumbel(sm, t, P.PARTS, P.vocab_b, P.TOK, P.STV, P.out,
+                 i, (i == NC - 1) ? 1 : 0, ncur, MP);
+    __threadfence(); gg.sync();
   }
 }
 
@@ -789,7 +989,6 @@
   float* out = (float*)d_out;
 
   dim3 thr(256);
-  dim3 thr512(512);
   const size_t NEED = 234889216ull;
 
   if (ws_size >= NEED) {
@@ -845,58 +1044,45 @@
     k_gemm<<<dim3(16, 16), thr, 0, stream>>>(BOSW, ca_wo, BOSb, nullptr, NB * NBOS, ND, ND, 0);
     k_out_init<<<dim3(NB), thr, 0, stream>>>(out);
 
-    k_build_ln<<<dim3(1024), thr, 0, stream>>>(BOSb, pos_emb, tok_emb, TOK, STV,
-                                               ln1_w, ln1_b, X, Hh, Hl, 0, NBOS);
+    k_build_ln<<<dim3(1024), thr, 0, stream>>>(BOSb, ln1_w, ln1_b, X, Hh, Hl);
     for (int l = 0; l < NL; ++l) {
-      k_g3<2><<<dim3(24, 8, 1), thr512, 0, stream>>>(Hh, Hl, WqH[l], WqL[l], nullptr, QKVh, QKVl,
-                                                     1024, 3072, 1024, 1024);
+      k_g3<2><<<dim3(24, 8, 1), thr, 0, stream>>>(Hh, Hl, WqH[l], WqL[l], nullptr, QKVh, QKVl,
+                                                  1024, 3072, 1024, 1024);
       k_copy_kv<<<dim3(1024), thr, 0, stream>>>(QKVh, QKVl, KVh[l], KVl[l]);
       k_attn16p<<<dim3(NB * NH), thr, 0, stream>>>(QKVh, QKVl, rel_bias + (size_t)l * (2 * NS - 1) * NH,
                                                    Hh, Hl, NBOS);
-      k_g3<0><<<dim3(8, 8, 3), thr512, 0, stream>>>(Hh, Hl, WaH[l], WaL[l], PARTS, nullptr, nullptr,
-                                                    1024, 1024, 1024, 352);
+      k_g3<0><<<dim3(8, 8, 3), thr, 0, stream>>>(Hh, Hl, WaH[l], WaL[l], PARTS, nullptr, nullptr,
+                                                 1024, 1024, 1024, 352);
       k_red_ln<1><<<dim3(1024), thr, 0, stream>>>(PARTS, X, ln2_w + l * ND, ln2_b + l * ND, Hh, Hl, 1024);
-      k_g3<1><<<dim3(32, 8, 1), thr512, 0, stream>>>(Hh, Hl, W1H[l], W1L[l], nullptr, Mh, Ml,
-                                                     1024, 4096, 1024, 1024);
-      k_g3<0><<<dim3(8, 8, 3), thr512, 0, stream>>>(Mh, Ml, W2H[l], W2L[l], PARTS, nullptr, nullptr,
-                                                    1024, 1024, 2048, 704);
+      k_g3<1><<<dim3(32, 8, 1), thr, 0, stream>>>(Hh, Hl, W1H[l], W1L[l], nullptr, Mh, Ml,
+                                                  1024, 4096, 1024, 1024);
+      k_g3<0><<<dim3(8, 8, 3), thr, 0, stream>>>(Mh, Ml, W2H[l], W2L[l], PARTS, nullptr, nullptr,
+                                                 1024, 1024, 2048, 704);
       if (l < NL - 1)
         k_red_ln<1><<<dim3(1024), thr, 0, stream>>>(PARTS, X, ln1_w + (l + 1) * ND, ln1_b + (l + 1) * ND,
                                                     Hh, Hl, 1024);
     }
 
-    for (int i = 0; i < NC; ++i) {
-      const int ncur = i + 1;
-      const int Mv = NB * ncur;
-      const int MP = (Mv + 127) & ~127;
-      const int gy = MP / 128;
-
-      k_build_ln_c<<<dim3(Mv), thr, 0, stream>>>(pos_emb, tok_emb, TOK, STV,
-                                                 ln1_w, ln1_b, X, Hh, Hl, i, ncur);
-      for (int l = 0; l < NL; ++l) {
-        k_g3<2><<<dim3(24, gy, 1), thr512, 0, stream>>>(Hh, Hl, WqH[l], WqL[l], nullptr, QKVh, QKVl,
-                                                        MP, 3072, 1024, 1024);
-        k_attn16c<<<dim3(NB * NH), thr, 0, stream>>>(QKVh, QKVl, KVh[l], KVl[l],
-                                                     rel_bias + (size_t)l * (2 * NS - 1) * NH,
-                                                     Hh, Hl, ncur);
-        k_g3<0><<<dim3(8, gy, 3), thr512, 0, stream>>>(Hh, Hl, WaH[l], WaL[l], PARTS, nullptr, nullptr,
-                                                       MP, 1024, 1024, 352);
-        k_red_ln<1><<<dim3(Mv), thr, 0, stream>>>(PARTS, X, ln2_w + l * ND, ln2_b + l * ND, Hh, Hl, MP);
-        k_g3<1><<<dim3(32, gy, 1), thr512, 0, stream>>>(Hh, Hl, W1H[l], W1L[l], nullptr, Mh, Ml,
-                                                        MP, 4096, 1024, 1024);
-        k_g3<0><<<dim3(8, gy, 3), thr512, 0, stream>>>(Mh, Ml, W2H[l], W2L[l], PARTS, nullptr, nullptr,
-                                                       MP, 1024, 2048, 704);
-        if (l < NL - 1)
-          k_red_ln<1><<<dim3(Mv), thr, 0, stream>>>(PARTS, X, ln1_w + (l + 1) * ND, ln1_b + (l + 1) * ND,
-                                                    Hh, Hl, MP);
-        else
-          k_red_ln<0><<<dim3(Mv), thr, 0, stream>>>(PARTS, X, lnf_w, lnf_b, Hh, Hl, MP);
-      }
-      k_g3<0><<<dim3(8, gy, 3), thr512, 0, stream>>>(Hh, Hl, WvH, WvL, PARTS, nullptr, nullptr,
-                                                     MP, 1024, 1024, 352);
-      k_gumbel_t<1><<<dim3(Mv), thr, 0, stream>>>(PARTS, vocab_b, TOK, STV, out, i,
-                                                  (i == NC - 1) ? 1 : 0, ncur, MP);
-    }
+    MegaP P;
+    P.WqH0 = WqH[0]; P.WqH1 = WqH[1]; P.WqH2 = WqH[2]; P.WqH3 = WqH[3];
+    P.WqL0 = WqL[0]; P.WqL1 = WqL[1]; P.WqL2 = WqL[2]; P.WqL3 = WqL[3];
+    P.WaH0 = WaH[0]; P.WaH1 = WaH[1]; P.WaH2 = WaH[2]; P.WaH3 = WaH[3];
+    P.WaL0 = WaL[0]; P.WaL1 = WaL[1]; P.WaL2 = WaL[2]; P.WaL3 = WaL[3];
+    P.W1H0 = W1H[0]; P.W1H1 = W1H[1]; P.W1H2 = W1H[2]; P.W1H3 = W1H[3];
+    P.W1L0 = W1L[0]; P.W1L1 = W1L[1]; P.W1L2 = W1L[2]; P.W1L3 = W1L[3];
+    P.W2H0 = W2H[0]; P.W2H1 = W2H[1]; P.W2H2 = W2H[2]; P.W2H3 = W2H[3];
+    P.W2L0 = W2L[0]; P.W2L1 = W2L[1]; P.W2L2 = W2L[2]; P.W2L3 = W2L[3];
+    P.WvH = WvH; P.WvL = WvL;
+    P.KVh0 = KVh[0]; P.KVh1 = KVh[1]; P.KVh2 = KVh[2]; P.KVh3 = KVh[3];
+    P.KVl0 = KVl[0]; P.KVl1 = KVl[1]; P.KVl2 = KVl[2]; P.KVl3 = KVl[3];
+    P.Hh = Hh; P.Hl = Hl; P.X = X; P.QKVh = QKVh; P.QKVl = QKVl;
+    P.PARTS = PARTS; P.Mh = Mh; P.Ml = Ml;
+    P.ln1_w = ln1_w; P.ln1_b = ln1_b; P.ln2_w = ln2_w; P.ln2_b = ln2_b;
+    P.lnf_w = lnf_w; P.lnf_b = lnf_b; P.vocab_b = vocab_b;
+    P.rel_bias = rel_bias; P.pos_emb = pos_emb; P.tok_emb = tok_emb;
+    P.STV = STV; P.TOK = TOK; P.out = out;
+    void* kargs[] = { (void*)&P };
+    hipLaunchCooperativeKernel((void*)k_mega, dim3(256), dim3(256), kargs, 0, stream);
     return;
   }
 
@@ -942,7 +1128,6 @@
     }
     k_lnf<<<dim3(NB * NC), thr, 0, stream>>>(X, lnf_w, lnf_b, HL);
     k_gemm<<<dim3(16, 14), thr, 0, stream>>>(HL, vocab_w, LG, vocab_b, NB * NC, NV, ND, 2);
-    k_gumbel_t<0><<<dim3(NB * NC), thr, 0, stream>>>(LG, nullptr, TOK, STV, out, i,
-                                                     (i == NC - 1) ? 1 : 0, NC, 896);
-  }
-}
+    k_gumbel_f<<<dim3(NB * NC), thr, 0, stream>>>(LG, TOK, STV, out, i, (i == NC - 1) ? 1 : 0);
+  }
+}
```

After: 33.33 ms. +276.5%, slower.
